# Kernel tuning notes

Hardware: AMD Instinct MI355X
Metric: run time of the kernel (lower is better)

## Reference

```python
import jax, jax.numpy as jnp
import numpy as np

N_IMG, N_CAP, N_REG, N_WORD = 64, 64, 36, 20
EMBED, SIM = 1024, 256
RCAR_STEP = 3          # rar_step=3, rcr_step=2, alv_step=3
T2I_SMOOTH = 9.0
EPS = 1e-8


def l2norm(x):
    return x / (jnp.linalg.norm(x, axis=-1, keepdims=True) + EPS)


def xavier(key, shape):
    fan_in, fan_out = shape[-1], shape[-2]
    r = float(np.sqrt(6.0 / (fan_in + fan_out)))
    return jax.random.uniform(key, shape, jnp.float32, -r, r)


def cross_attention(query, context, matrix, smooth):
    # query: (B, Q, D), context: (B, S, D); matrix broadcasts over query; smooth scalar or (B,Q,1)
    q = query * matrix
    attn = jnp.einsum('bsd,bqd->bsq', context, q)          # (B, S, Q)
    attn = jax.nn.leaky_relu(attn, 0.1)
    attn = l2norm(attn)                                     # normalize over Q
    attn = jnp.swapaxes(attn, 1, 2)                         # (B, Q, S)
    attn = jax.nn.softmax(attn * smooth, axis=2)
    wcontext = jnp.einsum('bqs,bsd->bqd', attn, context)    # (B, Q, D)
    return l2norm(wcontext)


def setup_inputs() -> dict:
    key = jax.random.key(0)
    ks = jax.random.split(key, 12)
    inp = {}
    inp['img_emb'] = jax.random.normal(ks[0], (N_IMG, N_REG, EMBED), jnp.float32)
    inp['cap_emb'] = jax.random.normal(ks[1], (N_CAP, N_WORD, EMBED), jnp.float32)
    inp['cap_lens'] = jnp.full((N_CAP,), N_WORD, dtype=jnp.int32)
    # Alignment_vector: Linear(embed -> sim), 3 steps
    inp['alv_w'] = xavier(ks[2], (RCAR_STEP, SIM, EMBED))
    inp['alv_b'] = jnp.zeros((RCAR_STEP, SIM), jnp.float32)
    # Aggregation_regulator: q/k Linear(sim->sim), v Linear(sim->1), 3 steps
    inp['rar_qw'] = xavier(ks[3], (RCAR_STEP, SIM, SIM))
    inp['rar_qb'] = jnp.zeros((RCAR_STEP, SIM), jnp.float32)
    inp['rar_kw'] = xavier(ks[4], (RCAR_STEP, SIM, SIM))
    inp['rar_kb'] = jnp.zeros((RCAR_STEP, SIM), jnp.float32)
    inp['rar_vw'] = xavier(ks[5], (RCAR_STEP, 1, SIM))
    inp['rar_vb'] = jnp.zeros((RCAR_STEP, 1), jnp.float32)
    # Correpondence_regulator: smooth MLP sim->sim//2->1, matrix MLP sim->2*sim->embed, 2 steps
    inp['rcr_sw1'] = xavier(ks[6], (RCAR_STEP - 1, SIM // 2, SIM))
    inp['rcr_sb1'] = jnp.zeros((RCAR_STEP - 1, SIM // 2), jnp.float32)
    inp['rcr_sw2'] = xavier(ks[7], (RCAR_STEP - 1, 1, SIM // 2))
    inp['rcr_sb2'] = jnp.zeros((RCAR_STEP - 1, 1), jnp.float32)
    inp['rcr_mw1'] = xavier(ks[8], (RCAR_STEP - 1, 2 * SIM, SIM))
    inp['rcr_mb1'] = jnp.zeros((RCAR_STEP - 1, 2 * SIM), jnp.float32)
    inp['rcr_mw2'] = xavier(ks[9], (RCAR_STEP - 1, EMBED, 2 * SIM))
    inp['rcr_mb2'] = jnp.zeros((RCAR_STEP - 1, EMBED), jnp.float32)
    # sim_eval_w: Linear(sim -> 1)
    inp['eval_w'] = xavier(ks[10], (1, SIM))
    inp['eval_b'] = jnp.zeros((1,), jnp.float32)
    return inp


def _forward(img_emb, cap_emb,
             alv_w, alv_b,
             rar_qw, rar_qb, rar_kw, rar_kb, rar_vw, rar_vb,
             rcr_sw1, rcr_sb1, rcr_sw2, rcr_sb2, rcr_mw1, rcr_mb1, rcr_mw2, rcr_mb2,
             eval_w, eval_b):
    n_img = img_emb.shape[0]

    def per_caption(cap_i):                       # cap_i: (L, D)
        query = jnp.broadcast_to(cap_i[None], (n_img,) + cap_i.shape)  # t2i: text is query
        context = img_emb                                               # (n_img, S, D)
        matrix = jnp.ones((EMBED,), cap_i.dtype)
        smooth = jnp.asarray(T2I_SMOOTH, cap_i.dtype)
        sim_hig = None
        for m in range(RCAR_STEP):
            # Alignment_vector (dropout is inference-mode identity)
            wctx = cross_attention(query, context, matrix, smooth)
            sim_rep = (query - wctx) ** 2
            sim_mid = l2norm(jnp.einsum('bqd,sd->bqs', sim_rep, alv_w[m]) + alv_b[m])  # (B,Q,SIM)
            if m == 0:
                sim_hig = sim_mid.mean(axis=1)                                          # (B,SIM)
            if m < RCAR_STEP - 1:
                # Correpondence_regulator
                hm = jnp.tanh(jnp.einsum('bqs,ts->bqt', sim_mid, rcr_mw1[m]) + rcr_mb1[m])
                mm = jnp.einsum('bqt,dt->bqd', hm, rcr_mw2[m]) + rcr_mb2[m]
                matrix = jnp.clip(jnp.tanh(mm) + matrix, -1.0, 1.0)                     # (B,Q,D)
                hs = jnp.tanh(jnp.einsum('bqs,ts->bqt', sim_mid, rcr_sw1[m]) + rcr_sb1[m])
                ss = jnp.einsum('bqt,ot->bqo', hs, rcr_sw2[m]) + rcr_sb2[m]
                smooth = jax.nn.relu(ss + smooth)                                       # (B,Q,1)
            # Aggregation_regulator
            mid_k = jnp.tanh(jnp.einsum('bqs,ts->bqt', sim_mid, rar_kw[m]) + rar_kb[m])
            hig_q = jnp.tanh(sim_hig @ rar_qw[m].T + rar_qb[m])[:, None, :]             # (B,1,SIM)
            w = jnp.einsum('bqs,os->bqo', mid_k * hig_q, rar_vw[m]) + rar_vb[m]         # (B,Q,1)
            w = jax.nn.softmax(w[..., 0], axis=1)
            sim_hig = l2norm(jnp.einsum('bq,bqs->bs', w, sim_mid))
        sim_i = jax.nn.sigmoid(sim_hig @ eval_w.T + eval_b)                             # (B,1)
        return sim_i[:, 0]

    sims = jax.vmap(per_caption)(cap_emb)        # (n_cap, n_img)
    return sims.T                                 # (n_img, n_cap) == torch.cat(sim_all, 1)


def reference(img_emb, cap_emb, cap_lens,
              alv_w, alv_b,
              rar_qw, rar_qb, rar_kw, rar_kb, rar_vw, rar_vb,
              rcr_sw1, rcr_sb1, rcr_sw2, rcr_sb2, rcr_mw1, rcr_mb1, rcr_mw2, rcr_mb2,
              eval_w, eval_b):
    # cap_lens are all equal to N_WORD (constant-length captions), so the per-caption
    # slice cap_emb[i, :n_word] is the full row and the loop vectorizes exactly.
    del cap_lens
    return _forward(img_emb, cap_emb, alv_w, alv_b,
                    rar_qw, rar_qb, rar_kw, rar_kb, rar_vw, rar_vb,
                    rcr_sw1, rcr_sb1, rcr_sw2, rcr_sb2, rcr_mw1, rcr_mb1, rcr_mw2, rcr_mb2,
                    eval_w, eval_b)
```

## Files before the change

### kernel.cpp

```cpp
#include <hip/hip_runtime.h>
#include <math.h>

#define NIMG 64
#define NCAP 64
#define NREG 36
#define NWORD 20
#define EMBED 1024
#define SIMDIM 256
#define H1 512
#define HSD 128
#define EPS 1e-8f

#define QSTR 1032
#define SMSTR 264
#define PSTR 72
#define ATSTR 37

typedef unsigned short u16t;
typedef __bf16 bf8 __attribute__((ext_vector_type(8)));
typedef short  s8i __attribute__((ext_vector_type(8)));
typedef float  f4  __attribute__((ext_vector_type(4)));

__device__ __forceinline__ float wsum(float v) {
#pragma unroll
  for (int o = 32; o > 0; o >>= 1) v += __shfl_xor(v, o);
  return v;
}
__device__ __forceinline__ float wmax(float v) {
#pragma unroll
  for (int o = 32; o > 0; o >>= 1) v = fmaxf(v, __shfl_xor(v, o));
  return v;
}
__device__ __forceinline__ float ftanh(float x) {
  x = fminf(fmaxf(x, -15.f), 15.f);
  float e = __expf(2.f * x);
  return (e - 1.f) / (e + 1.f);
}
__device__ __forceinline__ float d4(float4 a, float4 b) {
  return a.x*b.x + a.y*b.y + a.z*b.z + a.w*b.w;
}
__device__ __forceinline__ u16t f2bf(float f) {
  unsigned u = __float_as_uint(f);
  u += 0x7FFFu + ((u >> 16) & 1u);
  return (u16t)(u >> 16);
}
__device__ __forceinline__ float bf2f(u16t h) { return __uint_as_float(((unsigned)h) << 16); }
__device__ __forceinline__ bf8 zero8() {
  s8i z = {0,0,0,0,0,0,0,0};
  return __builtin_bit_cast(bf8, z);
}
#define MFMA16(a, b, c) __builtin_amdgcn_mfma_f32_16x16x32_bf16((a), (b), (c), 0, 0, 0)

#define WS_ALV   0u
#define WS_KW    786432u
#define WS_MW1   983040u
#define WS_MW2   1245184u
#define WS_SW1   2293760u
#define WS_IMG   2359296u
#define WS_CTXT  4718592u
#define WS_END   8912896u
#define N_CVT    4718592u

#define OFFB_MAT    17825792ull
#define OFFB_SMID   (OFFB_MAT + 83886080ull)
#define OFFB_SHIG   (OFFB_SMID + 41943040ull)
#define OFFB_SMOOTH (OFFB_SHIG + 4194304ull)
#define WS_FULL_BYTES (OFFB_SMOOTH + 327680ull)
#define OFFB_SREP   (OFFB_SMOOTH + 327680ull)
#define OFFB_HQU    (OFFB_SREP + 167772160ull)
#define OFFB_LOG    (OFFB_HQU + 4194304ull)
#define WS_FULL2_BYTES (OFFB_LOG + 327680ull)

__global__ void cvt_kernel(const float* __restrict__ alv, const float* __restrict__ kw,
                           const float* __restrict__ mw1, const float* __restrict__ mw2,
                           const float* __restrict__ sw1, const float* __restrict__ img,
                           u16t* __restrict__ ws) {
  for (unsigned i = blockIdx.x * blockDim.x + threadIdx.x; i < N_CVT; i += gridDim.x * blockDim.x) {
    unsigned o = i; float v;
    if (o < 786432u) v = alv[o];
    else if ((o -= 786432u) < 196608u) v = kw[o];
    else if ((o -= 196608u) < 262144u) v = mw1[o];
    else if ((o -= 262144u) < 1048576u) v = mw2[o];
    else if ((o -= 1048576u) < 65536u) v = sw1[o];
    else { o -= 65536u; v = img[o]; }
    ws[i] = f2bf(v);
  }
}

__global__ void ctxt_kernel(const float* __restrict__ img, u16t* __restrict__ ctxT) {
  __shared__ float tile[36 * 65];
  int b = blockIdx.x;
  int im = b >> 4, dt = (b & 15) * 64;
  const float* src = img + (size_t)im * 36 * 1024 + dt;
  for (int e = threadIdx.x; e < 36 * 64; e += 256) {
    int s = e >> 6, dd = e & 63;
    tile[s * 65 + dd] = src[s * 1024 + dd];
  }
  __syncthreads();
  u16t* dst = ctxT + (size_t)im * 65536 + dt * 64;
  for (int o = threadIdx.x; o < 4096; o += 256) {
    int dd = o >> 6, sp = o & 63;
    dst[dd * 64 + sp] = (sp < 36) ? f2bf(tile[sp * 65 + dd]) : (u16t)0;
  }
}

__global__ __launch_bounds__(512, 4) void simenc_ka(
    const float* __restrict__ cap_emb,
    const u16t* __restrict__ ws,
    const signed char* __restrict__ mat_g,
    const float* __restrict__ smooth_g,
    u16t* __restrict__ srep_g,
    int m)
{
  __shared__ __attribute__((aligned(16))) u16t qsrep[NWORD * QSTR];
  __shared__ __attribute__((aligned(16))) u16t p_bf[NWORD * PSTR];
  __shared__ float attnT[NWORD * ATSTR];
  __shared__ float colscale[36];
  __shared__ float smoothq[NWORD];
  __shared__ float red[8 * NWORD];
  __shared__ float rq[NWORD];

  const int tid = threadIdx.x;
  const int lane = tid & 63;
  const int wv = tid >> 6;
  const int lr = lane & 15;
  const int lg = lane >> 4;
  const int koff = lg * 8;

  const int xcd = blockIdx.x & 7;
  const int j_  = blockIdx.x >> 3;
  const int img = xcd * 8 + (j_ & 7);
  const int cap = j_ >> 3;
  const int pid = img * NCAP + cap;

  const float* qry  = cap_emb + (size_t)cap * (NWORD * EMBED);
  const u16t* imgW  = ws + WS_IMG + (size_t)img * (NREG * EMBED);
  const u16t* ctxTW = ws + WS_CTXT + (size_t)img * (EMBED * 64);

  if (tid < NWORD)
    smoothq[tid] = (m == 0) ? 9.0f : smooth_g[(size_t)pid * 20 + tid];
  __syncthreads();

  if (m == 0) {
#pragma unroll 4
    for (int q = 0; q < NWORD; ++q) {
      qsrep[q * QSTR + tid] = f2bf(qry[q * 1024 + tid]);
      qsrep[q * QSTR + 512 + tid] = f2bf(qry[q * 1024 + 512 + tid]);
    }
  } else {
    const signed char* mg = mat_g + (size_t)pid * 20480;
#pragma unroll 4
    for (int q = 0; q < NWORD; ++q) {
      float mv0 = (float)mg[q * 1024 + tid] * (1.f / 127.f);
      float mv1 = (float)mg[q * 1024 + 512 + tid] * (1.f / 127.f);
      qsrep[q * QSTR + tid] = f2bf(qry[q * 1024 + tid] * mv0);
      qsrep[q * QSTR + 512 + tid] = f2bf(qry[q * 1024 + 512 + tid] * mv1);
    }
  }
  __syncthreads();

  if (wv < 6) {
    int q0 = (wv & 1) * 16, s0 = (wv >> 1) * 16;
    int ari = q0 + lr; bool am = ari >= NWORD; int ar = am ? 0 : ari;
    int bri = s0 + lr; bool bm = bri >= NREG;  int br = bm ? 0 : bri;
    const u16t* ap = qsrep + ar * QSTR + koff;
    const u16t* bp = imgW + (size_t)br * 1024 + koff;
    f4 acc0 = {0.f,0.f,0.f,0.f}, acc1 = {0.f,0.f,0.f,0.f};
#pragma unroll 2
    for (int kk = 0; kk < 32; kk += 2) {
      bf8 a0 = *(const bf8*)(ap + kk * 32);       if (am) a0 = zero8();
      bf8 b0 = *(const bf8*)(bp + kk * 32);       if (bm) b0 = zero8();
      bf8 a1 = *(const bf8*)(ap + (kk + 1) * 32); if (am) a1 = zero8();
      bf8 b1 = *(const bf8*)(bp + (kk + 1) * 32); if (bm) b1 = zero8();
      acc0 = MFMA16(a0, b0, acc0);
      acc1 = MFMA16(a1, b1, acc1);
    }
    f4 acc = acc0 + acc1;
#pragma unroll
    for (int r = 0; r < 4; ++r) {
      int q = q0 + lg * 4 + r, s = s0 + lr;
      if (q < NWORD && s < NREG) {
        float x = acc[r];
        attnT[q * ATSTR + s] = (x > 0.f) ? x : 0.1f * x;
      }
    }
  }
  __syncthreads();

  if (tid < NREG) {
    float ss = 0.f;
#pragma unroll
    for (int q = 0; q < NWORD; ++q) { float v = attnT[q * ATSTR + tid]; ss += v * v; }
    colscale[tid] = 1.f / (sqrtf(ss) + EPS);
  }
  __syncthreads();

#pragma unroll
  for (int pass = 0; pass < 3; ++pass) {
    int q = wv + pass * 8;
    if (q < NWORD) {
      float x = (lane < NREG)
              ? attnT[q * ATSTR + lane] * colscale[lane] * smoothq[q] : -1e30f;
      float mx = wmax(x);
      float e = (lane < NREG) ? __expf(x - mx) : 0.f;
      float s = wsum(e);
      p_bf[q * PSTR + lane] = f2bf(e / s);
    }
  }
  __syncthreads();

  {
    bf8 pa[2][2];
#pragma unroll
    for (int kk = 0; kk < 2; ++kk) {
      pa[0][kk] = *(const bf8*)(p_bf + lr * PSTR + kk * 32 + koff);
      pa[1][kk] = (16 + lr < NWORD)
                ? *(const bf8*)(p_bf + (16 + lr) * PSTR + kk * 32 + koff) : zero8();
    }
    float s2[8];
#pragma unroll
    for (int i = 0; i < 8; ++i) s2[i] = 0.f;
#pragma unroll
    for (int nt = 0; nt < 8; ++nt) {
      int d0 = wv * 128 + nt * 16;
      const u16t* bp = ctxTW + (size_t)(d0 + lr) * 64 + koff;
      bf8 b0 = *(const bf8*)(bp);
      bf8 b1 = *(const bf8*)(bp + 32);
      int d = d0 + lr;
#pragma unroll
      for (int m2 = 0; m2 < 2; ++m2) {
        f4 acc = {0.f,0.f,0.f,0.f};
        acc = MFMA16(pa[m2][0], b0, acc);
        acc = MFMA16(pa[m2][1], b1, acc);
#pragma unroll
        for (int r = 0; r < 4; ++r) {
          int q = m2 * 16 + lg * 4 + r;
          s2[m2 * 4 + r] += acc[r] * acc[r];
          if (q < NWORD) qsrep[q * QSTR + d] = f2bf(acc[r]);
        }
      }
    }
#pragma unroll
    for (int o = 1; o < 16; o <<= 1)
#pragma unroll
      for (int i = 0; i < 8; ++i) s2[i] += __shfl_xor(s2[i], o);
    if (lr == 0) {
#pragma unroll
      for (int r = 0; r < 4; ++r) red[wv * 20 + lg * 4 + r] = s2[r];
      if (lg == 0)
#pragma unroll
        for (int r = 0; r < 4; ++r) red[wv * 20 + 16 + r] = s2[4 + r];
    }
    __syncthreads();
    if (tid < NWORD) {
      float s = 0.f;
#pragma unroll
      for (int w = 0; w < 8; ++w) s += red[w * 20 + tid];
      rq[tid] = 1.f / (sqrtf(s) + EPS);
    }
    __syncthreads();
#pragma unroll
    for (int nt = 0; nt < 8; ++nt) {
      int d = wv * 128 + nt * 16 + lr;
#pragma unroll
      for (int m2 = 0; m2 < 2; ++m2)
#pragma unroll
        for (int r = 0; r < 4; ++r) {
          int q = m2 * 16 + lg * 4 + r;
          if (q < NWORD) {
            float wn = bf2f(qsrep[q * QSTR + d]) * rq[q];
            float t = qry[q * 1024 + d] - wn;
            qsrep[q * QSTR + d] = f2bf(t * t);
          }
        }
    }
  }
  __syncthreads();

  {
    u16t* sp = srep_g + (size_t)pid * 20480;
#pragma unroll 4
    for (int i = tid; i < 20480; i += 512) {
      int row = i >> 10, col = i & 1023;
      sp[i] = qsrep[row * QSTR + col];
    }
  }
}

__global__ __launch_bounds__(1024, 4) void simenc_kf(
    const float* __restrict__ alv_b,
    const u16t* __restrict__ ws,
    const u16t* __restrict__ srep_g,
    u16t* __restrict__ smid_g,
    float* __restrict__ shig_g,
    int m)
{
  __shared__ __attribute__((aligned(16))) u16t smid_l[80 * SMSTR];
  __shared__ float red[16 * 80];
  __shared__ float rq80[80];

  const int tid = threadIdx.x;
  const int lane = tid & 63;
  const int wv = tid >> 6;
  const int lr = lane & 15;
  const int lg = lane >> 4;
  const int koff = lg * 8;

  const int pid0 = blockIdx.x * 4;
  const u16t* alvW = ws + WS_ALV + (size_t)m * (SIMDIM * EMBED);
  const u16t* srepB = srep_g + (size_t)pid0 * 20480;

  int t_ = wv * 16 + lr;
  f4 acc[5];
#pragma unroll
  for (int mt = 0; mt < 5; ++mt) acc[mt] = (f4){0,0,0,0};
#pragma unroll 2
  for (int kk = 0; kk < 32; ++kk) {
    bf8 b = *(const bf8*)(alvW + (size_t)t_ * 1024 + kk * 32 + koff);
#pragma unroll
    for (int mt = 0; mt < 5; ++mt) {
      bf8 a = *(const bf8*)(srepB + (size_t)(mt * 16 + lr) * 1024 + kk * 32 + koff);
      acc[mt] = MFMA16(a, b, acc[mt]);
    }
  }
  float bias = alv_b[m * SIMDIM + t_];
  float p[20];
#pragma unroll
  for (int mt = 0; mt < 5; ++mt)
#pragma unroll
    for (int r = 0; r < 4; ++r) {
      acc[mt][r] += bias;
      p[mt * 4 + r] = acc[mt][r] * acc[mt][r];
    }
#pragma unroll
  for (int o = 1; o < 16; o <<= 1)
#pragma unroll
    for (int i = 0; i < 20; ++i) p[i] += __shfl_xor(p[i], o);
  if (lr == 0)
#pragma unroll
    for (int mt = 0; mt < 5; ++mt)
#pragma unroll
      for (int r = 0; r < 4; ++r)
        red[wv * 80 + mt * 16 + lg * 4 + r] = p[mt * 4 + r];
  __syncthreads();
  if (tid < 80) {
    float s = 0.f;
#pragma unroll
    for (int w = 0; w < 16; ++w) s += red[w * 80 + tid];
    rq80[tid] = 1.f / (sqrtf(s) + EPS);
  }
  __syncthreads();
#pragma unroll
  for (int mt = 0; mt < 5; ++mt)
#pragma unroll
    for (int r = 0; r < 4; ++r) {
      int rb = mt * 16 + lg * 4 + r;
      float v = acc[mt][r] * rq80[rb];
      u16t hv = f2bf(v);
      smid_g[(size_t)(pid0 * 20 + rb) * 256 + t_] = hv;
      smid_l[rb * SMSTR + t_] = hv;
    }
  if (m == 0) {
    __syncthreads();
    int col = tid & 255, pp = tid >> 8;
    float s = 0.f;
#pragma unroll
    for (int q = 0; q < NWORD; ++q) s += bf2f(smid_l[(pp * 20 + q) * SMSTR + col]);
    shig_g[(size_t)(pid0 + pp) * 256 + col] = s * (1.f / NWORD);
  }
}

__global__ __launch_bounds__(1024) void simenc_kh(
    const float* __restrict__ rar_qw, const float* __restrict__ rar_qb,
    const float* __restrict__ rar_vw,
    const float* __restrict__ shig_g, float* __restrict__ hqu_g, int m)
{
  int idx = blockIdx.x * 1024 + threadIdx.x;
  int pid = idx >> 8, t = idx & 255;
  const float4* sh = (const float4*)(shig_g + (size_t)pid * 256);
  const float4* wq = (const float4*)(rar_qw + ((size_t)m * SIMDIM + t) * SIMDIM);
  float acc = 0.f;
#pragma unroll 8
  for (int i = 0; i < SIMDIM / 4; ++i) acc += d4(wq[i], sh[i]);
  hqu_g[idx] = ftanh(acc + rar_qb[m * SIMDIM + t]) * rar_vw[m * SIMDIM + t];
}

__global__ __launch_bounds__(1024, 4) void simenc_kr(
    const float* __restrict__ rar_kb, const float* __restrict__ rar_vb,
    const float* __restrict__ sb1, const float* __restrict__ sw2, const float* __restrict__ sb2,
    const u16t* __restrict__ ws,
    const u16t* __restrict__ smid_g, const float* __restrict__ hqu_g,
    float* __restrict__ logits_g, float* __restrict__ smooth_g,
    int m)
{
  __shared__ float red[16 * 80];

  const int tid = threadIdx.x;
  const int lane = tid & 63;
  const int wv = tid >> 6;
  const int lr = lane & 15;
  const int lg = lane >> 4;
  const int koff = lg * 8;

  const int pid0 = blockIdx.x * 4;
  const u16t* kwW  = ws + WS_KW  + (size_t)m * (SIMDIM * SIMDIM);
  const u16t* sw1W = ws + WS_SW1 + (size_t)m * (HSD * SIMDIM);
  const u16t* smidB = smid_g + (size_t)pid0 * 5120;

  {
    int t_ = wv * 16 + lr;
    f4 acc[5];
#pragma unroll
    for (int mt = 0; mt < 5; ++mt) acc[mt] = (f4){0,0,0,0};
#pragma unroll 2
    for (int kk = 0; kk < 8; ++kk) {
      bf8 b = *(const bf8*)(kwW + (size_t)t_ * 256 + kk * 32 + koff);
#pragma unroll
      for (int mt = 0; mt < 5; ++mt) {
        bf8 a = *(const bf8*)(smidB + (size_t)(mt * 16 + lr) * 256 + kk * 32 + koff);
        acc[mt] = MFMA16(a, b, acc[mt]);
      }
    }
    float kb = rar_kb[m * SIMDIM + t_];
    float p[20];
#pragma unroll
    for (int mt = 0; mt < 5; ++mt)
#pragma unroll
      for (int r = 0; r < 4; ++r) {
        int rb = mt * 16 + lg * 4 + r;
        float hq = hqu_g[(size_t)(pid0 + rb / 20) * 256 + t_];
        p[mt * 4 + r] = ftanh(acc[mt][r] + kb) * hq;
      }
#pragma unroll
    for (int o = 1; o < 16; o <<= 1)
#pragma unroll
      for (int i = 0; i < 20; ++i) p[i] += __shfl_xor(p[i], o);
    if (lr == 0)
#pragma unroll
      for (int mt = 0; mt < 5; ++mt)
#pragma unroll
        for (int r = 0; r < 4; ++r)
          red[wv * 80 + mt * 16 + lg * 4 + r] = p[mt * 4 + r];
  }
  __syncthreads();
  if (tid < 80) {
    float s = 0.f;
#pragma unroll
    for (int w = 0; w < 16; ++w) s += red[w * 80 + tid];
    logits_g[(size_t)pid0 * 20 + tid] = s + rar_vb[m];
  }

  if (m < 2) {
    __syncthreads();
    if (wv < 8) {
      int j_ = wv * 16 + lr;
      f4 acc[5];
#pragma unroll
      for (int mt = 0; mt < 5; ++mt) acc[mt] = (f4){0,0,0,0};
#pragma unroll 2
      for (int kk = 0; kk < 8; ++kk) {
        bf8 b = *(const bf8*)(sw1W + (size_t)j_ * 256 + kk * 32 + koff);
#pragma unroll
        for (int mt = 0; mt < 5; ++mt) {
          bf8 a = *(const bf8*)(smidB + (size_t)(mt * 16 + lr) * 256 + kk * 32 + koff);
          acc[mt] = MFMA16(a, b, acc[mt]);
        }
      }
      float b1 = sb1[m * HSD + j_];
      float s2v = sw2[m * HSD + j_];
      float p[20];
#pragma unroll
      for (int mt = 0; mt < 5; ++mt)
#pragma unroll
        for (int r = 0; r < 4; ++r)
          p[mt * 4 + r] = ftanh(acc[mt][r] + b1) * s2v;
#pragma unroll
      for (int o = 1; o < 16; o <<= 1)
#pragma unroll
        for (int i = 0; i < 20; ++i) p[i] += __shfl_xor(p[i], o);
      if (lr == 0)
#pragma unroll
        for (int mt = 0; mt < 5; ++mt)
#pragma unroll
          for (int r = 0; r < 4; ++r)
            red[wv * 80 + mt * 16 + lg * 4 + r] = p[mt * 4 + r];
    }
    __syncthreads();
    if (tid < 80) {
      float s = 0.f;
#pragma unroll
      for (int w = 0; w < 8; ++w) s += red[w * 80 + tid];
      float old = (m == 0) ? 9.0f : smooth_g[(size_t)pid0 * 20 + tid];
      smooth_g[(size_t)pid0 * 20 + tid] = fmaxf(0.f, s + sb2[m] + old);
    }
  }
}

__global__ __launch_bounds__(256) void simenc_ki(
    const float* __restrict__ eval_w, const float* __restrict__ eval_b,
    const u16t* __restrict__ smid_g, const float* __restrict__ logits_g,
    float* __restrict__ shig_g, float* __restrict__ out, int m)
{
  __shared__ float wsm[NWORD];
  __shared__ float sh[SIMDIM];
  __shared__ float red4[4];
  __shared__ float rsig;

  const int pid = blockIdx.x;
  const int tid = threadIdx.x;

  if (tid < 64) {
    float v = (tid < NWORD) ? logits_g[(size_t)pid * 20 + tid] : -1e30f;
    float mx = wmax(v);
    float e = (tid < NWORD) ? __expf(v - mx) : 0.f;
    float s = wsum(e);
    if (tid < NWORD) wsm[tid] = e / s;
  }
  __syncthreads();
  {
    const u16t* sm = smid_g + (size_t)pid * 5120 + tid;
    float a = 0.f;
#pragma unroll
    for (int q = 0; q < NWORD; ++q) a += wsm[q] * bf2f(sm[q * 256]);
    sh[tid] = a;
  }
  __syncthreads();
  {
    float v = sh[tid];
    float ss = wsum(v * v);
    if ((tid & 63) == 0) red4[tid >> 6] = ss;
  }
  __syncthreads();
  if (tid == 0) rsig = 1.f / (sqrtf(red4[0] + red4[1] + red4[2] + red4[3]) + EPS);
  __syncthreads();
  if (m < 2) {
    shig_g[(size_t)pid * 256 + tid] = sh[tid] * rsig;
  } else if (tid < 64) {
    float4 s4 = ((const float4*)sh)[tid];
    float4 w4 = ((const float4*)eval_w)[tid];
    float v = wsum(d4(s4, w4)) * rsig;
    if (tid == 0) out[pid] = 1.f / (1.f + __expf(-(v + eval_b[0])));
  }
}

__global__ __launch_bounds__(1024, 4) void simenc_k2(
    const float* __restrict__ mb1, const float* __restrict__ mb2,
    const u16t* __restrict__ ws,
    const u16t* __restrict__ smid_g, signed char* __restrict__ mat_g,
    int m)
{
  __shared__ __attribute__((aligned(16))) u16t hm_l[80 * 512];
  __shared__ __attribute__((aligned(16))) signed char mat_l[80 * 1024];

  const int tid = threadIdx.x;
  const int lane = tid & 63;
  const int wv = tid >> 6;
  const int lr = lane & 15;
  const int lg = lane >> 4;
  const int koff = lg * 8;

  const int pid0 = blockIdx.x * 4;
  const u16t* mw1W = ws + WS_MW1 + (size_t)m * (H1 * SIMDIM);
  const u16t* mw2W = ws + WS_MW2 + (size_t)m * (EMBED * H1);
  const u16t* smidB = smid_g + (size_t)pid0 * 5120;

#pragma unroll
  for (int nt = 0; nt < 2; ++nt) {
    int j0 = (wv * 2 + nt) * 16;
    f4 acc[5];
#pragma unroll
    for (int mt = 0; mt < 5; ++mt) acc[mt] = (f4){0,0,0,0};
#pragma unroll 2
    for (int kk = 0; kk < 8; ++kk) {
      bf8 b = *(const bf8*)(mw1W + (size_t)(j0 + lr) * 256 + kk * 32 + koff);
#pragma unroll
      for (int mt = 0; mt < 5; ++mt) {
        bf8 a = *(const bf8*)(smidB + (size_t)(mt * 16 + lr) * 256 + kk * 32 + koff);
        acc[mt] = MFMA16(a, b, acc[mt]);
      }
    }
    int j = j0 + lr;
    float bias = mb1[m * H1 + j];
#pragma unroll
    for (int mt = 0; mt < 5; ++mt)
#pragma unroll
      for (int r = 0; r < 4; ++r) {
        int rb = mt * 16 + lg * 4 + r;
        unsigned byteoff = (unsigned)rb * 1024u
                         + (((unsigned)j * 2u) ^ (((unsigned)rb & 7u) << 4));
        *(u16t*)((char*)hm_l + byteoff) = f2bf(ftanh(acc[mt][r] + bias));
      }
  }
  __syncthreads();

#pragma unroll
  for (int nt = 0; nt < 4; ++nt) {
    int d0 = (wv * 4 + nt) * 16;
    f4 acc[5];
#pragma unroll
    for (int mt = 0; mt < 5; ++mt) acc[mt] = (f4){0,0,0,0};
#pragma unroll 2
    for (int kk = 0; kk < 16; ++kk) {
      bf8 b = *(const bf8*)(mw2W + (size_t)(d0 + lr) * 512 + kk * 32 + koff);
#pragma unroll
      for (int mt = 0; mt < 5; ++mt) {
        int rb = mt * 16 + lr;
        unsigned byteoff = (unsigned)rb * 1024u
                         + (((unsigned)(kk * 64 + lg * 16)) ^ (((unsigned)rb & 7u) << 4));
        bf8 a = *(const bf8*)((const char*)hm_l + byteoff);
        acc[mt] = MFMA16(a, b, acc[mt]);
      }
    }
    int d = d0 + lr;
    float bias = mb2[m * EMBED + d];
#pragma unroll
    for (int mt = 0; mt < 5; ++mt)
#pragma unroll
      for (int r = 0; r < 4; ++r) {
        int rb = mt * 16 + lg * 4 + r;
        float v = ftanh(acc[mt][r] + bias);
        mat_l[rb * 1024 + d] = (signed char)__float2int_rn(v * 127.f);
      }
  }
  __syncthreads();

  {
    signed char* matB = mat_g + (size_t)pid0 * 20480;
#pragma unroll
    for (int i = 0; i < 5; ++i) {
      int off = i * 16384 + tid * 16;
      int4 sv = *(const int4*)(mat_l + off);
      int4 ov;
      if (m > 0) ov = *(const int4*)(matB + off);
      const signed char* svb = (const signed char*)&sv;
      const signed char* ovb = (const signed char*)&ov;
      int4 res;
      signed char* rsb = (signed char*)&res;
#pragma unroll
      for (int b = 0; b < 16; ++b) {
        float v = (float)svb[b] * (1.f / 127.f);
        float mo = (m == 0) ? 1.f : (float)ovb[b] * (1.f / 127.f);
        float mn = fminf(fmaxf(v + mo, -1.f), 1.f);
        rsb[b] = (signed char)__float2int_rn(mn * 127.f);
      }
      *(int4*)(matB + off) = res;
    }
  }
}

__global__ __launch_bounds__(512, 4) void simenc_k1f(
    const float* __restrict__ cap_emb,
    const float* __restrict__ alv_b,
    const float* __restrict__ rar_qw, const float* __restrict__ rar_qb,
    const float* __restrict__ rar_kb,
    const float* __restrict__ rar_vw, const float* __restrict__ rar_vb,
    const float* __restrict__ sb1, const float* __restrict__ sw2, const float* __restrict__ sb2,
    const float* __restrict__ eval_w, const float* __restrict__ eval_b,
    const u16t* __restrict__ ws,
    signed char* __restrict__ mat_g, u16t* __restrict__ smid_g,
    float* __restrict__ shig_g, float* __restrict__ smooth_g,
    int m, float* __restrict__ out)
{
  __shared__ __attribute__((aligned(16))) u16t qsrep[NWORD * QSTR];
  __shared__ __attribute__((aligned(16))) u16t smidb[NWORD * SMSTR];
  __shared__ __attribute__((aligned(16))) u16t p_bf[NWORD * PSTR];
  __shared__ float attnT[NWORD * ATSTR];
  __shared__ float colscale[36];
  __shared__ float smoothq[NWORD];
  __shared__ float sim_hig[SIMDIM];
  __shared__ float red[8 * NWORD];
  __shared__ float rq[NWORD];
  __shared__ float logits_s[NWORD];
  __shared__ float wsm[NWORD];
  __shared__ float ssig_s;

  const int tid = threadIdx.x;
  const int lane = tid & 63;
  const int wv = tid >> 6;
  const int lr = lane & 15;
  const int lg = lane >> 4;
  const int koff = lg * 8;

  const int xcd = blockIdx.x & 7;
  const int j_  = blockIdx.x >> 3;
  const int img = xcd * 8 + (j_ & 7);
  const int cap = j_ >> 3;
  const int pid = img * NCAP + cap;

  const float* qry  = cap_emb + (size_t)cap * (NWORD * EMBED);
  const u16t* imgW  = ws + WS_IMG + (size_t)img * (NREG * EMBED);
  const u16t* ctxTW = ws + WS_CTXT + (size_t)img * (EMBED * 64);
  const u16t* alvW  = ws + WS_ALV + (size_t)m * (SIMDIM * EMBED);
  const u16t* kwW   = ws + WS_KW  + (size_t)m * (SIMDIM * SIMDIM);
  const u16t* sw1W  = ws + WS_SW1 + (size_t)m * (HSD * SIMDIM);

  if (tid < NWORD)
    smoothq[tid] = (m == 0) ? 9.0f : smooth_g[(size_t)pid * 20 + tid];
  if (m > 0 && tid < 256)
    sim_hig[tid] = shig_g[(size_t)pid * 256 + tid];
  __syncthreads();

  if (m == 0) {
#pragma unroll 4
    for (int q = 0; q < NWORD; ++q) {
      qsrep[q * QSTR + tid] = f2bf(qry[q * 1024 + tid]);
      qsrep[q * QSTR + 512 + tid] = f2bf(qry[q * 1024 + 512 + tid]);
    }
  } else {
    const signed char* mg = mat_g + (size_t)pid * 20480;
#pragma unroll 4
    for (int q = 0; q < NWORD; ++q) {
      float mv0 = (float)mg[q * 1024 + tid] * (1.f / 127.f);
      float mv1 = (float)mg[q * 1024 + 512 + tid] * (1.f / 127.f);
      qsrep[q * QSTR + tid] = f2bf(qry[q * 1024 + tid] * mv0);
      qsrep[q * QSTR + 512 + tid] = f2bf(qry[q * 1024 + 512 + tid] * mv1);
    }
  }
  __syncthreads();

  if (wv < 6) {
    int q0 = (wv & 1) * 16, s0 = (wv >> 1) * 16;
    int ari = q0 + lr; bool am = ari >= NWORD; int ar = am ? 0 : ari;
    int bri = s0 + lr; bool bm = bri >= NREG;  int br = bm ? 0 : bri;
    const u16t* ap = qsrep + ar * QSTR + koff;
    const u16t* bp = imgW + (size_t)br * 1024 + koff;
    f4 acc0 = {0.f,0.f,0.f,0.f}, acc1 = {0.f,0.f,0.f,0.f};
#pragma unroll 2
    for (int kk = 0; kk < 32; kk += 2) {
      bf8 a0 = *(const bf8*)(ap + kk * 32);       if (am) a0 = zero8();
      bf8 b0 = *(const bf8*)(bp + kk * 32);       if (bm) b0 = zero8();
      bf8 a1 = *(const bf8*)(ap + (kk + 1) * 32); if (am) a1 = zero8();
      bf8 b1 = *(const bf8*)(bp + (kk + 1) * 32); if (bm) b1 = zero8();
      acc0 = MFMA16(a0, b0, acc0);
      acc1 = MFMA16(a1, b1, acc1);
    }
    f4 acc = acc0 + acc1;
#pragma unroll
    for (int r = 0; r < 4; ++r) {
      int q = q0 + lg * 4 + r, s = s0 + lr;
      if (q < NWORD && s < NREG) {
        float x = acc[r];
        attnT[q * ATSTR + s] = (x > 0.f) ? x : 0.1f * x;
      }
    }
  }
  __syncthreads();

  if (tid < NREG) {
    float ss = 0.f;
#pragma unroll
    for (int q = 0; q < NWORD; ++q) { float v = attnT[q * ATSTR + tid]; ss += v * v; }
    colscale[tid] = 1.f / (sqrtf(ss) + EPS);
  }
  __syncthreads();

#pragma unroll
  for (int pass = 0; pass < 3; ++pass) {
    int q = wv + pass * 8;
    if (q < NWORD) {
      float x = (lane < NREG)
              ? attnT[q * ATSTR + lane] * colscale[lane] * smoothq[q] : -1e30f;
      float mx = wmax(x);
      float e = (lane < NREG) ? __expf(x - mx) : 0.f;
      float s = wsum(e);
      p_bf[q * PSTR + lane] = f2bf(e / s);
    }
  }
  __syncthreads();

  {
    bf8 pa[2][2];
#pragma unroll
    for (int kk = 0; kk < 2; ++kk) {
      pa[0][kk] = *(const bf8*)(p_bf + lr * PSTR + kk * 32 + koff);
      pa[1][kk] = (16 + lr < NWORD)
                ? *(const bf8*)(p_bf + (16 + lr) * PSTR + kk * 32 + koff) : zero8();
    }
    float s2[8];
#pragma unroll
    for (int i = 0; i < 8; ++i) s2[i] = 0.f;
#pragma unroll
    for (int nt = 0; nt < 8; ++nt) {
      int d0 = wv * 128 + nt * 16;
      const u16t* bp = ctxTW + (size_t)(d0 + lr) * 64 + koff;
      bf8 b0 = *(const bf8*)(bp);
      bf8 b1 = *(const bf8*)(bp + 32);
      int d = d0 + lr;
#pragma unroll
      for (int m2 = 0; m2 < 2; ++m2) {
        f4 acc = {0.f,0.f,0.f,0.f};
        acc = MFMA16(pa[m2][0], b0, acc);
        acc = MFMA16(pa[m2][1], b1, acc);
#pragma unroll
        for (int r = 0; r < 4; ++r) {
          int q = m2 * 16 + lg * 4 + r;
          s2[m2 * 4 + r] += acc[r] * acc[r];
          if (q < NWORD) qsrep[q * QSTR + d] = f2bf(acc[r]);
        }
      }
    }
#pragma unroll
    for (int o = 1; o < 16; o <<= 1)
#pragma unroll
      for (int i = 0; i < 8; ++i) s2[i] += __shfl_xor(s2[i], o);
    if (lr == 0) {
#pragma unroll
      for (int r = 0; r < 4; ++r) red[wv * 20 + lg * 4 + r] = s2[r];
      if (lg == 0)
#pragma unroll
        for (int r = 0; r < 4; ++r) red[wv * 20 + 16 + r] = s2[4 + r];
    }
    __syncthreads();
    if (tid < NWORD) {
      float s = 0.f;
#pragma unroll
      for (int w = 0; w < 8; ++w) s += red[w * 20 + tid];
      rq[tid] = 1.f / (sqrtf(s) + EPS);
    }
    __syncthreads();
#pragma unroll
    for (int nt = 0; nt < 8; ++nt) {
      int d = wv * 128 + nt * 16 + lr;
#pragma unroll
      for (int m2 = 0; m2 < 2; ++m2)
#pragma unroll
        for (int r = 0; r < 4; ++r) {
          int q = m2 * 16 + lg * 4 + r;
          if (q < NWORD) {
            float wn = bf2f(qsrep[q * QSTR + d]) * rq[q];
            float t = qry[q * 1024 + d] - wn;
            qsrep[q * QSTR + d] = f2bf(t * t);
          }
        }
    }
  }
  __syncthreads();

  {
    int t0 = wv * 32 + lr;
    const u16t* bp0 = alvW + (size_t)t0 * 1024 + koff;
    const u16t* bp1 = bp0 + 16 * 1024;
    int ari = 16 + lr; bool am = ari >= NWORD; int ar = am ? 0 : ari;
    f4 a00 = {0,0,0,0}, a01 = {0,0,0,0}, a10 = {0,0,0,0}, a11 = {0,0,0,0};
#pragma unroll 2
    for (int kk = 0; kk < 32; ++kk) {
      bf8 b0 = *(const bf8*)(bp0 + kk * 32);
      bf8 b1 = *(const bf8*)(bp1 + kk * 32);
      bf8 x0 = *(const bf8*)(qsrep + lr * QSTR + kk * 32 + koff);
      bf8 x1 = *(const bf8*)(qsrep + ar * QSTR + kk * 32 + koff); if (am) x1 = zero8();
      a00 = MFMA16(x0, b0, a00);
      a01 = MFMA16(x1, b0, a01);
      a10 = MFMA16(x0, b1, a10);
      a11 = MFMA16(x1, b1, a11);
    }
    float bias0 = alv_b[m * SIMDIM + t0];
    float bias1 = alv_b[m * SIMDIM + t0 + 16];
    float s2[8];
#pragma unroll
    for (int r = 0; r < 4; ++r) {
      a00[r] += bias0; a10[r] += bias1;
      s2[r] = a00[r] * a00[r] + a10[r] * a10[r];
    }
#pragma unroll
    for (int r = 0; r < 4; ++r) {
      a01[r] += bias0; a11[r] += bias1;
      s2[4 + r] = (lg == 0) ? a01[r] * a01[r] + a11[r] * a11[r] : 0.f;
    }
#pragma unroll
    for (int o = 1; o < 16; o <<= 1)
#pragma unroll
      for (int i = 0; i < 8; ++i) s2[i] += __shfl_xor(s2[i], o);
    if (lr == 0) {
#pragma unroll
      for (int r = 0; r < 4; ++r) red[wv * 20 + lg * 4 + r] = s2[r];
      if (lg == 0)
#pragma unroll
        for (int r = 0; r < 4; ++r) red[wv * 20 + 16 + r] = s2[4 + r];
    }
    __syncthreads();
    if (tid < NWORD) {
      float s = 0.f;
#pragma unroll
      for (int w = 0; w < 8; ++w) s += red[w * 20 + tid];
      rq[tid] = 1.f / (sqrtf(s) + EPS);
    }
    __syncthreads();
    u16t* sg = smid_g + (size_t)pid * 5120;
#pragma unroll
    for (int r = 0; r < 4; ++r) {
      int q = lg * 4 + r;
      float v0 = a00[r] * rq[q], v1 = a10[r] * rq[q];
      u16t h0 = f2bf(v0), h1 = f2bf(v1);
      ((float*)(qsrep + q * QSTR + 512))[t0] = v0;
      ((float*)(qsrep + q * QSTR + 512))[t0 + 16] = v1;
      smidb[q * SMSTR + t0] = h0;
      smidb[q * SMSTR + t0 + 16] = h1;
      sg[q * 256 + t0] = h0;
      sg[q * 256 + t0 + 16] = h1;
    }
    if (lg == 0)
#pragma unroll
      for (int r = 0; r < 4; ++r) {
        int q = 16 + r;
        float v0 = a01[r] * rq[q], v1 = a11[r] * rq[q];
        u16t h0 = f2bf(v0), h1 = f2bf(v1);
        ((float*)(qsrep + q * QSTR + 512))[t0] = v0;
        ((float*)(qsrep + q * QSTR + 512))[t0 + 16] = v1;
        smidb[q * SMSTR + t0] = h0;
        smidb[q * SMSTR + t0 + 16] = h1;
        sg[q * 256 + t0] = h0;
        sg[q * 256 + t0 + 16] = h1;
      }
  }
  __syncthreads();

  if (m == 0 && tid < 256) {
    float s = 0.f;
#pragma unroll
    for (int q = 0; q < NWORD; ++q) s += ((const float*)(qsrep + q * QSTR + 512))[tid];
    sim_hig[tid] = s * (1.f / NWORD);
  }
  __syncthreads();

  if (m < 2) {
    {
      int j0 = wv * 16;
      int ari = 16 + lr; bool am = ari >= NWORD; int ar = am ? 0 : ari;
      f4 h0 = {0,0,0,0}, h1 = {0,0,0,0};
#pragma unroll 2
      for (int kk = 0; kk < 8; ++kk) {
        bf8 b = *(const bf8*)(sw1W + (size_t)(j0 + lr) * 256 + kk * 32 + koff);
        bf8 x0 = *(const bf8*)(smidb + lr * SMSTR + kk * 32 + koff);
        bf8 x1 = *(const bf8*)(smidb + ar * SMSTR + kk * 32 + koff); if (am) x1 = zero8();
        h0 = MFMA16(x0, b, h0);
        h1 = MFMA16(x1, b, h1);
      }
      int j = j0 + lr;
      float bias = sb1[m * HSD + j];
      float s2v = sw2[m * HSD + j];
      float part[8];
#pragma unroll
      for (int r = 0; r < 4; ++r) part[r] = ftanh(h0[r] + bias) * s2v;
#pragma unroll
      for (int r = 0; r < 4; ++r) part[4 + r] = (lg == 0) ? ftanh(h1[r] + bias) * s2v : 0.f;
#pragma unroll
      for (int o = 1; o < 16; o <<= 1)
#pragma unroll
        for (int i = 0; i < 8; ++i) part[i] += __shfl_xor(part[i], o);
      if (lr == 0) {
#pragma unroll
        for (int r = 0; r < 4; ++r) red[wv * 20 + lg * 4 + r] = part[r];
        if (lg == 0)
#pragma unroll
          for (int r = 0; r < 4; ++r) red[wv * 20 + 16 + r] = part[4 + r];
      }
    }
    __syncthreads();
    if (tid < NWORD) {
      float s = 0.f;
#pragma unroll
      for (int w = 0; w < 8; ++w) s += red[w * 20 + tid];
      smooth_g[(size_t)pid * 20 + tid] = fmaxf(0.f, s + sb2[m] + smoothq[tid]);
    }
    __syncthreads();
  }

  {
    int ari = 16 + lr; bool am = ari >= NWORD; int ar = am ? 0 : ari;
    float part[8];
#pragma unroll
    for (int i = 0; i < 8; ++i) part[i] = 0.f;
#pragma unroll
    for (int h = 0; h < 2; ++h) {
      int t_ = wv * 32 + h * 16 + lr;
      const float4* wq = (const float4*)(rar_qw + ((size_t)m * SIMDIM + t_) * SIMDIM);
      const float4* sh = (const float4*)sim_hig;
      float hacc = 0.f;
#pragma unroll 2
      for (int i = 0; i < SIMDIM / 4; ++i) hacc += d4(wq[i], sh[i]);
      float hq = ftanh(hacc + rar_qb[m * SIMDIM + t_]) * rar_vw[m * SIMDIM + t_];

      f4 k0 = {0,0,0,0}, k1v = {0,0,0,0};
#pragma unroll 2
      for (int kk = 0; kk < 8; ++kk) {
        bf8 b = *(const bf8*)(kwW + (size_t)t_ * 256 + kk * 32 + koff);
        bf8 x0 = *(const bf8*)(smidb + lr * SMSTR + kk * 32 + koff);
        bf8 x1 = *(const bf8*)(smidb + ar * SMSTR + kk * 32 + koff); if (am) x1 = zero8();
        k0 = MFMA16(x0, b, k0);
        k1v = MFMA16(x1, b, k1v);
      }
      float kb = rar_kb[m * SIMDIM + t_];
#pragma unroll
      for (int r = 0; r < 4; ++r) part[r] += ftanh(k0[r] + kb) * hq;
      if (lg == 0)
#pragma unroll
        for (int r = 0; r < 4; ++r) part[4 + r] += ftanh(k1v[r] + kb) * hq;
    }
#pragma unroll
    for (int o = 1; o < 16; o <<= 1)
#pragma unroll
      for (int i = 0; i < 8; ++i) part[i] += __shfl_xor(part[i], o);
    if (lr == 0) {
#pragma unroll
      for (int r = 0; r < 4; ++r) red[wv * 20 + lg * 4 + r] = part[r];
      if (lg == 0)
#pragma unroll
        for (int r = 0; r < 4; ++r) red[wv * 20 + 16 + r] = part[4 + r];
    }
  }
  __syncthreads();
  if (tid < NWORD) {
    float s = 0.f;
#pragma unroll
    for (int w = 0; w < 8; ++w) s += red[w * 20 + tid];
    logits_s[tid] = s + rar_vb[m];
  }
  __syncthreads();
  if (tid < 64) {
    float v = (tid < NWORD) ? logits_s[tid] : -1e30f;
    float mx = wmax(v);
    float e = (tid < NWORD) ? __expf(v - mx) : 0.f;
    float s = wsum(e);
    if (tid < NWORD) wsm[tid] = e / s;
  }
  __syncthreads();
  if (tid < 256) {
    float a = 0.f;
#pragma unroll
    for (int q = 0; q < NWORD; ++q) a += wsm[q] * ((const float*)(qsrep + q * QSTR + 512))[tid];
    sim_hig[tid] = a;
  }
  __syncthreads();
  if (tid < 64) {
    float4 v = ((const float4*)sim_hig)[tid];
    float s = wsum(d4(v, v));
    if (tid == 0) ssig_s = 1.f / (sqrtf(s) + EPS);
  }
  __syncthreads();

  if (m < 2) {
    if (tid < 256)
      shig_g[(size_t)pid * 256 + tid] = sim_hig[tid] * ssig_s;
  } else {
    if (tid < 64) {
      float4 s4v = ((const float4*)sim_hig)[tid];
      float4 w4v = ((const float4*)eval_w)[tid];
      float v = wsum(d4(s4v, w4v)) * ssig_s;
      if (tid == 0)
        out[pid] = 1.f / (1.f + __expf(-(v + eval_b[0])));
    }
  }
}

extern "C" void kernel_launch(void* const* d_in, const int* in_sizes, int n_in,
                              void* d_out, int out_size, void* d_ws, size_t ws_size,
                              hipStream_t stream) {
  (void)in_sizes; (void)n_in; (void)out_size;
  u16t* ws = (u16t*)d_ws;

  signed char* mat_g = (signed char*)d_ws + OFFB_MAT;
  u16t*  smid_g   = (u16t*)((char*)d_ws + OFFB_SMID);
  float* shig_g   = (float*)((char*)d_ws + OFFB_SHIG);
  float* smooth_g = (float*)((char*)d_ws + OFFB_SMOOTH);

  cvt_kernel<<<2048, 1024, 0, stream>>>(
      (const float*)d_in[3],  (const float*)d_in[7],  (const float*)d_in[15],
      (const float*)d_in[17], (const float*)d_in[11], (const float*)d_in[0], ws);
  ctxt_kernel<<<1024, 256, 0, stream>>>((const float*)d_in[0], ws + WS_CTXT);

  if (ws_size >= (size_t)WS_FULL2_BYTES) {
    u16t*  srep_g   = (u16t*)((char*)d_ws + OFFB_SREP);
    float* hqu_g    = (float*)((char*)d_ws + OFFB_HQU);
    float* logits_g = (float*)((char*)d_ws + OFFB_LOG);

    for (int m = 0; m < 3; ++m) {
      simenc_ka<<<NIMG * NCAP, 512, 0, stream>>>(
          (const float*)d_in[1], ws, mat_g, smooth_g, srep_g, m);
      simenc_kf<<<NIMG * NCAP / 4, 1024, 0, stream>>>(
          (const float*)d_in[4], ws, srep_g, smid_g, shig_g, m);
      simenc_kh<<<1024, 1024, 0, stream>>>(
          (const float*)d_in[5], (const float*)d_in[6], (const float*)d_in[9],
          shig_g, hqu_g, m);
      simenc_kr<<<NIMG * NCAP / 4, 1024, 0, stream>>>(
          (const float*)d_in[8], (const float*)d_in[10],
          (const float*)d_in[12], (const float*)d_in[13], (const float*)d_in[14],
          ws, smid_g, hqu_g, logits_g, smooth_g, m);
      simenc_ki<<<NIMG * NCAP, 256, 0, stream>>>(
          (const float*)d_in[19], (const float*)d_in[20],
          smid_g, logits_g, shig_g, (float*)d_out, m);
      if (m < 2)
        simenc_k2<<<NIMG * NCAP / 4, 1024, 0, stream>>>(
            (const float*)d_in[16], (const float*)d_in[18],
            ws, smid_g, mat_g, m);
    }
  } else {
    for (int m = 0; m < 3; ++m) {
      simenc_k1f<<<NIMG * NCAP, 512, 0, stream>>>(
          (const float*)d_in[1],  (const float*)d_in[4],
          (const float*)d_in[5],  (const float*)d_in[6],  (const float*)d_in[8],
          (const float*)d_in[9],  (const float*)d_in[10],
          (const float*)d_in[12], (const float*)d_in[13], (const float*)d_in[14],
          (const float*)d_in[19], (const float*)d_in[20],
          ws, mat_g, smid_g, shig_g, smooth_g, m, (float*)d_out);
      if (m < 2)
        simenc_k2<<<NIMG * NCAP / 4, 1024, 0, stream>>>(
            (const float*)d_in[16], (const float*)d_in[18],
            ws, smid_g, mat_g, m);
    }
  }
}
```

Measured before the change: 3.513 ms.

## Fuse per-step pipeline into one persistent kernel with global scratch for query rep

Replaces the five-kernel per-step chain (ka, kf, kh, kr, ki) with one fused kernel, simenc_k1g. It launches 1024 blocks, and each block loops over 4 image-caption pairs, computing attention, the alignment vector, the smooth MLP, the regulator and the final sigmoid in one pass. The large shared query buffer is moved to a per-block global scratch area (srep_g). This frees shared memory for fp32 and bf16 sim_mid tiles and lets launch bounds rise to 8 blocks per CU. It removes kernel launches and global round trips for intermediates, at the cost of global-memory traffic for the query/residual buffer and heavier per-block serial work.

```diff
diff --git a/kernel.cpp b/kernel.cpp
--- a/kernel.cpp
+++ b/kernel.cpp
@@ -66,10 +66,8 @@
 #define OFFB_SHIG   (OFFB_SMID + 41943040ull)
 #define OFFB_SMOOTH (OFFB_SHIG + 4194304ull)
 #define WS_FULL_BYTES (OFFB_SMOOTH + 327680ull)
-#define OFFB_SREP   (OFFB_SMOOTH + 327680ull)
-#define OFFB_HQU    (OFFB_SREP + 167772160ull)
-#define OFFB_LOG    (OFFB_HQU + 4194304ull)
-#define WS_FULL2_BYTES (OFFB_LOG + 327680ull)
+#define OFFB_SREP   WS_FULL_BYTES
+#define WS_TIER_A   (OFFB_SREP + 41943040ull)
 
 __global__ void cvt_kernel(const float* __restrict__ alv, const float* __restrict__ kw,
                            const float* __restrict__ mw1, const float* __restrict__ mw2,
@@ -104,21 +102,32 @@
   }
 }
 
-__global__ __launch_bounds__(512, 4) void simenc_ka(
+__global__ __launch_bounds__(512, 8) void simenc_k1g(
     const float* __restrict__ cap_emb,
+    const float* __restrict__ alv_b,
+    const float* __restrict__ rar_qw, const float* __restrict__ rar_qb,
+    const float* __restrict__ rar_kb,
+    const float* __restrict__ rar_vw, const float* __restrict__ rar_vb,
+    const float* __restrict__ sb1, const float* __restrict__ sw2, const float* __restrict__ sb2,
+    const float* __restrict__ eval_w, const float* __restrict__ eval_b,
     const u16t* __restrict__ ws,
-    const signed char* __restrict__ mat_g,
-    const float* __restrict__ smooth_g,
+    signed char* __restrict__ mat_g, u16t* __restrict__ smid_g,
+    float* __restrict__ shig_g, float* __restrict__ smooth_g,
     u16t* __restrict__ srep_g,
-    int m)
+    int m, float* __restrict__ out)
 {
-  __shared__ __attribute__((aligned(16))) u16t qsrep[NWORD * QSTR];
+  __shared__ float smidf[NWORD * 256];
+  __shared__ __attribute__((aligned(16))) u16t smidb[NWORD * SMSTR];
   __shared__ __attribute__((aligned(16))) u16t p_bf[NWORD * PSTR];
   __shared__ float attnT[NWORD * ATSTR];
   __shared__ float colscale[36];
   __shared__ float smoothq[NWORD];
+  __shared__ float sim_hig[SIMDIM];
   __shared__ float red[8 * NWORD];
   __shared__ float rq[NWORD];
+  __shared__ float logits_s[NWORD];
+  __shared__ float wsm[NWORD];
+  __shared__ float ssig_s;
 
   const int tid = threadIdx.x;
   const int lane = tid & 63;
@@ -127,523 +136,374 @@
   const int lg = lane >> 4;
   const int koff = lg * 8;
 
-  const int xcd = blockIdx.x & 7;
-  const int j_  = blockIdx.x >> 3;
-  const int img = xcd * 8 + (j_ & 7);
-  const int cap = j_ >> 3;
-  const int pid = img * NCAP + cap;
-
-  const float* qry  = cap_emb + (size_t)cap * (NWORD * EMBED);
-  const u16t* imgW  = ws + WS_IMG + (size_t)img * (NREG * EMBED);
-  const u16t* ctxTW = ws + WS_CTXT + (size_t)img * (EMBED * 64);
-
-  if (tid < NWORD)
-    smoothq[tid] = (m == 0) ? 9.0f : smooth_g[(size_t)pid * 20 + tid];
-  __syncthreads();
-
-  if (m == 0) {
+  u16t* srp = srep_g + (size_t)blockIdx.x * 20480;
+
+  for (int c = 0; c < 4; ++c) {
+    int v = blockIdx.x + (c << 10);
+    int xcd = v & 7, j_ = v >> 3;
+    int img = xcd * 8 + (j_ & 7);
+    int cap = j_ >> 3;
+    int pid = img * NCAP + cap;
+
+    const float* qry  = cap_emb + (size_t)cap * (NWORD * EMBED);
+    const u16t* imgW  = ws + WS_IMG + (size_t)img * (NREG * EMBED);
+    const u16t* ctxTW = ws + WS_CTXT + (size_t)img * (EMBED * 64);
+    const u16t* alvW  = ws + WS_ALV + (size_t)m * (SIMDIM * EMBED);
+    const u16t* kwW   = ws + WS_KW  + (size_t)m * (SIMDIM * SIMDIM);
+    const u16t* sw1W  = ws + WS_SW1 + (size_t)m * (HSD * SIMDIM);
+
+    __syncthreads();
+    if (tid < NWORD)
+      smoothq[tid] = (m == 0) ? 9.0f : smooth_g[(size_t)pid * 20 + tid];
+    if (m > 0 && tid < 256)
+      sim_hig[tid] = shig_g[(size_t)pid * 256 + tid];
+
+    {
+      int c0 = tid * 2;
+      if (m == 0) {
 #pragma unroll 4
-    for (int q = 0; q < NWORD; ++q) {
-      qsrep[q * QSTR + tid] = f2bf(qry[q * 1024 + tid]);
-      qsrep[q * QSTR + 512 + tid] = f2bf(qry[q * 1024 + 512 + tid]);
-    }
-  } else {
-    const signed char* mg = mat_g + (size_t)pid * 20480;
+        for (int q = 0; q < NWORD; ++q) {
+          float2 qv = *(const float2*)(qry + q * 1024 + c0);
+          unsigned pk = (unsigned)f2bf(qv.x) | ((unsigned)f2bf(qv.y) << 16);
+          *(unsigned*)(srp + q * 1024 + c0) = pk;
+        }
+      } else {
+        const signed char* mg = mat_g + (size_t)pid * 20480;
 #pragma unroll 4
-    for (int q = 0; q < NWORD; ++q) {
-      float mv0 = (float)mg[q * 1024 + tid] * (1.f / 127.f);
-      float mv1 = (float)mg[q * 1024 + 512 + tid] * (1.f / 127.f);
-      qsrep[q * QSTR + tid] = f2bf(qry[q * 1024 + tid] * mv0);
-      qsrep[q * QSTR + 512 + tid] = f2bf(qry[q * 1024 + 512 + tid] * mv1);
-    }
-  }
-  __syncthreads();
-
-  if (wv < 6) {
-    int q0 = (wv & 1) * 16, s0 = (wv >> 1) * 16;
-    int ari = q0 + lr; bool am = ari >= NWORD; int ar = am ? 0 : ari;
-    int bri = s0 + lr; bool bm = bri >= NREG;  int br = bm ? 0 : bri;
-    const u16t* ap = qsrep + ar * QSTR + koff;
-    const u16t* bp = imgW + (size_t)br * 1024 + koff;
-    f4 acc0 = {0.f,0.f,0.f,0.f}, acc1 = {0.f,0.f,0.f,0.f};
-#pragma unroll 2
-    for (int kk = 0; kk < 32; kk += 2) {
-      bf8 a0 = *(const bf8*)(ap + kk * 32);       if (am) a0 = zero8();
-      bf8 b0 = *(const bf8*)(bp + kk * 32);       if (bm) b0 = zero8();
-      bf8 a1 = *(const bf8*)(ap + (kk + 1) * 32); if (am) a1 = zero8();
-      bf8 b1 = *(const bf8*)(bp + (kk + 1) * 32); if (bm) b1 = zero8();
-      acc0 = MFMA16(a0, b0, acc0);
-      acc1 = MFMA16(a1, b1, acc1);
-    }
-    f4 acc = acc0 + acc1;
-#pragma unroll
-    for (int r = 0; r < 4; ++r) {
-      int q = q0 + lg * 4 + r, s = s0 + lr;
-      if (q < NWORD && s < NREG) {
-        float x = acc[r];
-        attnT[q * ATSTR + s] = (x > 0.f) ? x : 0.1f * x;
-      }
-    }
-  }
-  __syncthreads();
-
-  if (tid < NREG) {
-    float ss = 0.f;
-#pragma unroll
-    for (int q = 0; q < NWORD; ++q) { float v = attnT[q * ATSTR + tid]; ss += v * v; }
-    colscale[tid] = 1.f / (sqrtf(ss) + EPS);
-  }
-  __syncthreads();
-
-#pragma unroll
-  for (int pass = 0; pass < 3; ++pass) {
-    int q = wv + pass * 8;
-    if (q < NWORD) {
-      float x = (lane < NREG)
-              ? attnT[q * ATSTR + lane] * colscale[lane] * smoothq[q] : -1e30f;
-      float mx = wmax(x);
-      float e = (lane < NREG) ? __expf(x - mx) : 0.f;
-      float s = wsum(e);
-      p_bf[q * PSTR + lane] = f2bf(e / s);
-    }
-  }
-  __syncthreads();
-
-  {
-    bf8 pa[2][2];
-#pragma unroll
-    for (int kk = 0; kk < 2; ++kk) {
-      pa[0][kk] = *(const bf8*)(p_bf + lr * PSTR + kk * 32 + koff);
-      pa[1][kk] = (16 + lr < NWORD)
-                ? *(const bf8*)(p_bf + (16 + lr) * PSTR + kk * 32 + koff) : zero8();
-    }
-    float s2[8];
-#pragma unroll
-    for (int i = 0; i < 8; ++i) s2[i] = 0.f;
-#pragma unroll
-    for (int nt = 0; nt < 8; ++nt) {
-      int d0 = wv * 128 + nt * 16;
-      const u16t* bp = ctxTW + (size_t)(d0 + lr) * 64 + koff;
-      bf8 b0 = *(const bf8*)(bp);
-      bf8 b1 = *(const bf8*)(bp + 32);
-      int d = d0 + lr;
-#pragma unroll
-      for (int m2 = 0; m2 < 2; ++m2) {
-        f4 acc = {0.f,0.f,0.f,0.f};
-        acc = MFMA16(pa[m2][0], b0, acc);
-        acc = MFMA16(pa[m2][1], b1, acc);
+        for (int q = 0; q < NWORD; ++q) {
+          float2 qv = *(const float2*)(qry + q * 1024 + c0);
+          float m0 = (float)mg[q * 1024 + c0] * (1.f / 127.f);
+          float m1 = (float)mg[q * 1024 + c0 + 1] * (1.f / 127.f);
+          unsigned pk = (unsigned)f2bf(qv.x * m0) | ((unsigned)f2bf(qv.y * m1) << 16);
+          *(unsigned*)(srp + q * 1024 + c0) = pk;
+        }
+      }
+    }
+    __syncthreads();
+
+    if (wv < 6) {
+      int q0 = (wv & 1) * 16, s0 = (wv >> 1) * 16;
+      int ari = q0 + lr; bool am = ari >= NWORD; int ar = am ? 0 : ari;
+      int bri = s0 + lr; bool bm = bri >= NREG;  int br = bm ? 0 : bri;
+      const u16t* ap = srp + ar * 1024 + koff;
+      const u16t* bp = imgW + (size_t)br * 1024 + koff;
+      f4 acc0 = {0.f,0.f,0.f,0.f}, acc1 = {0.f,0.f,0.f,0.f};
+      for (int kk = 0; kk < 32; kk += 2) {
+        bf8 a0 = *(const bf8*)(ap + kk * 32);       if (am) a0 = zero8();
+        bf8 b0 = *(const bf8*)(bp + kk * 32);       if (bm) b0 = zero8();
+        bf8 a1 = *(const bf8*)(ap + (kk + 1) * 32); if (am) a1 = zero8();
+        bf8 b1 = *(const bf8*)(bp + (kk + 1) * 32); if (bm) b1 = zero8();
+        acc0 = MFMA16(a0, b0, acc0);
+        acc1 = MFMA16(a1, b1, acc1);
+      }
+      f4 acc = acc0 + acc1;
+#pragma unroll
+      for (int r = 0; r < 4; ++r) {
+        int q = q0 + lg * 4 + r, s = s0 + lr;
+        if (q < NWORD && s < NREG) {
+          float x = acc[r];
+          attnT[q * ATSTR + s] = (x > 0.f) ? x : 0.1f * x;
+        }
+      }
+    }
+    __syncthreads();
+
+    if (tid < NREG) {
+      float ss = 0.f;
+#pragma unroll
+      for (int q = 0; q < NWORD; ++q) { float vv = attnT[q * ATSTR + tid]; ss += vv * vv; }
+      colscale[tid] = 1.f / (sqrtf(ss) + EPS);
+    }
+    __syncthreads();
+
+#pragma unroll
+    for (int pass = 0; pass < 3; ++pass) {
+      int q = wv + pass * 8;
+      if (q < NWORD) {
+        float x = (lane < NREG)
+                ? attnT[q * ATSTR + lane] * colscale[lane] * smoothq[q] : -1e30f;
+        float mx = wmax(x);
+        float e = (lane < NREG) ? __expf(x - mx) : 0.f;
+        float s = wsum(e);
+        p_bf[q * PSTR + lane] = f2bf(e / s);
+      }
+    }
+    __syncthreads();
+
+    {
+      bf8 pa[2][2];
+#pragma unroll
+      for (int kk = 0; kk < 2; ++kk) {
+        pa[0][kk] = *(const bf8*)(p_bf + lr * PSTR + kk * 32 + koff);
+        pa[1][kk] = (16 + lr < NWORD)
+                  ? *(const bf8*)(p_bf + (16 + lr) * PSTR + kk * 32 + koff) : zero8();
+      }
+      float s2[8];
+#pragma unroll
+      for (int i = 0; i < 8; ++i) s2[i] = 0.f;
+      for (int nt = 0; nt < 8; ++nt) {
+        int d0 = wv * 128 + nt * 16;
+        const u16t* bp = ctxTW + (size_t)(d0 + lr) * 64 + koff;
+        bf8 b0 = *(const bf8*)(bp);
+        bf8 b1 = *(const bf8*)(bp + 32);
+        int d = d0 + lr;
+#pragma unroll
+        for (int m2 = 0; m2 < 2; ++m2) {
+          f4 acc = {0.f,0.f,0.f,0.f};
+          acc = MFMA16(pa[m2][0], b0, acc);
+          acc = MFMA16(pa[m2][1], b1, acc);
+#pragma unroll
+          for (int r = 0; r < 4; ++r) {
+            int q = m2 * 16 + lg * 4 + r;
+            s2[m2 * 4 + r] += acc[r] * acc[r];
+            if (q < NWORD) srp[q * 1024 + d] = f2bf(acc[r]);
+          }
+        }
+      }
+#pragma unroll
+      for (int o = 1; o < 16; o <<= 1)
+#pragma unroll
+        for (int i = 0; i < 8; ++i) s2[i] += __shfl_xor(s2[i], o);
+      if (lr == 0) {
+#pragma unroll
+        for (int r = 0; r < 4; ++r) red[wv * 20 + lg * 4 + r] = s2[r];
+        if (lg == 0)
+#pragma unroll
+          for (int r = 0; r < 4; ++r) red[wv * 20 + 16 + r] = s2[4 + r];
+      }
+      __syncthreads();
+      if (tid < NWORD) {
+        float s = 0.f;
+#pragma unroll
+        for (int w = 0; w < 8; ++w) s += red[w * 20 + tid];
+        rq[tid] = 1.f / (sqrtf(s) + EPS);
+      }
+      __syncthreads();
+      for (int nt = 0; nt < 8; ++nt) {
+        int d = wv * 128 + nt * 16 + lr;
+#pragma unroll
+        for (int m2 = 0; m2 < 2; ++m2)
+#pragma unroll
+          for (int r = 0; r < 4; ++r) {
+            int q = m2 * 16 + lg * 4 + r;
+            if (q < NWORD) {
+              float wn = bf2f(srp[q * 1024 + d]) * rq[q];
+              float t = qry[q * 1024 + d] - wn;
+              srp[q * 1024 + d] = f2bf(t * t);
+            }
+          }
+      }
+    }
+    __syncthreads();
+
+    {
+      int t0 = wv * 32 + lr;
+      const u16t* bp0 = alvW + (size_t)t0 * 1024 + koff;
+      const u16t* bp1 = bp0 + 16 * 1024;
+      int ari = 16 + lr; bool am = ari >= NWORD; int ar = am ? 0 : ari;
+      f4 a00 = {0,0,0,0}, a01 = {0,0,0,0}, a10 = {0,0,0,0}, a11 = {0,0,0,0};
+      for (int kk = 0; kk < 32; ++kk) {
+        bf8 b0 = *(const bf8*)(bp0 + kk * 32);
+        bf8 b1 = *(const bf8*)(bp1 + kk * 32);
+        bf8 x0 = *(const bf8*)(srp + lr * 1024 + kk * 32 + koff);
+        bf8 x1 = *(const bf8*)(srp + ar * 1024 + kk * 32 + koff); if (am) x1 = zero8();
+        a00 = MFMA16(x0, b0, a00);
+        a01 = MFMA16(x1, b0, a01);
+        a10 = MFMA16(x0, b1, a10);
+        a11 = MFMA16(x1, b1, a11);
+      }
+      float bias0 = alv_b[m * SIMDIM + t0];
+      float bias1 = alv_b[m * SIMDIM + t0 + 16];
+      float s2[8];
+#pragma unroll
+      for (int r = 0; r < 4; ++r) {
+        a00[r] += bias0; a10[r] += bias1;
+        s2[r] = a00[r] * a00[r] + a10[r] * a10[r];
+      }
+#pragma unroll
+      for (int r = 0; r < 4; ++r) {
+        a01[r] += bias0; a11[r] += bias1;
+        s2[4 + r] = (lg == 0) ? a01[r] * a01[r] + a11[r] * a11[r] : 0.f;
+      }
+#pragma unroll
+      for (int o = 1; o < 16; o <<= 1)
+#pragma unroll
+        for (int i = 0; i < 8; ++i) s2[i] += __shfl_xor(s2[i], o);
+      if (lr == 0) {
+#pragma unroll
+        for (int r = 0; r < 4; ++r) red[wv * 20 + lg * 4 + r] = s2[r];
+        if (lg == 0)
+#pragma unroll
+          for (int r = 0; r < 4; ++r) red[wv * 20 + 16 + r] = s2[4 + r];
+      }
+      __syncthreads();
+      if (tid < NWORD) {
+        float s = 0.f;
+#pragma unroll
+        for (int w = 0; w < 8; ++w) s += red[w * 20 + tid];
+        rq[tid] = 1.f / (sqrtf(s) + EPS);
+      }
+      __syncthreads();
+      u16t* sg = smid_g + (size_t)pid * 5120;
+#pragma unroll
+      for (int r = 0; r < 4; ++r) {
+        int q = lg * 4 + r;
+        float v0 = a00[r] * rq[q], v1 = a10[r] * rq[q];
+        u16t h0 = f2bf(v0), h1 = f2bf(v1);
+        smidf[q * 256 + t0] = v0;
+        smidf[q * 256 + t0 + 16] = v1;
+        smidb[q * SMSTR + t0] = h0;
+        smidb[q * SMSTR + t0 + 16] = h1;
+        sg[q * 256 + t0] = h0;
+        sg[q * 256 + t0 + 16] = h1;
+      }
+      if (lg == 0)
 #pragma unroll
         for (int r = 0; r < 4; ++r) {
-          int q = m2 * 16 + lg * 4 + r;
-          s2[m2 * 4 + r] += acc[r] * acc[r];
-          if (q < NWORD) qsrep[q * QSTR + d] = f2bf(acc[r]);
+          int q = 16 + r;
+          float v0 = a01[r] * rq[q], v1 = a11[r] * rq[q];
+          u16t h0 = f2bf(v0), h1 = f2bf(v1);
+          smidf[q * 256 + t0] = v0;
+          smidf[q * 256 + t0 + 16] = v1;
+          smidb[q * SMSTR + t0] = h0;
+          smidb[q * SMSTR + t0 + 16] = h1;
+          sg[q * 256 + t0] = h0;
+          sg[q * 256 + t0 + 16] = h1;
         }
-      }
-    }
-#pragma unroll
-    for (int o = 1; o < 16; o <<= 1)
-#pragma unroll
-      for (int i = 0; i < 8; ++i) s2[i] += __shfl_xor(s2[i], o);
-    if (lr == 0) {
-#pragma unroll
-      for (int r = 0; r < 4; ++r) red[wv * 20 + lg * 4 + r] = s2[r];
-      if (lg == 0)
-#pragma unroll
-        for (int r = 0; r < 4; ++r) red[wv * 20 + 16 + r] = s2[4 + r];
+    }
+    __syncthreads();
+
+    if (m == 0 && tid < 256) {
+      float s = 0.f;
+#pragma unroll
+      for (int q = 0; q < NWORD; ++q) s += smidf[q * 256 + tid];
+      sim_hig[tid] = s * (1.f / NWORD);
+    }
+    __syncthreads();
+
+    if (m < 2) {
+      {
+        int j0 = wv * 16;
+        int ari = 16 + lr; bool am = ari >= NWORD; int ar = am ? 0 : ari;
+        f4 h0 = {0,0,0,0}, h1 = {0,0,0,0};
+        for (int kk = 0; kk < 8; ++kk) {
+          bf8 b = *(const bf8*)(sw1W + (size_t)(j0 + lr) * 256 + kk * 32 + koff);
+          bf8 x0 = *(const bf8*)(smidb + lr * SMSTR + kk * 32 + koff);
+          bf8 x1 = *(const bf8*)(smidb + ar * SMSTR + kk * 32 + koff); if (am) x1 = zero8();
+          h0 = MFMA16(x0, b, h0);
+          h1 = MFMA16(x1, b, h1);
+        }
+        int j = j0 + lr;
+        float bias = sb1[m * HSD + j];
+        float s2v = sw2[m * HSD + j];
+        float part[8];
+#pragma unroll
+        for (int r = 0; r < 4; ++r) part[r] = ftanh(h0[r] + bias) * s2v;
+#pragma unroll
+        for (int r = 0; r < 4; ++r) part[4 + r] = (lg == 0) ? ftanh(h1[r] + bias) * s2v : 0.f;
+#pragma unroll
+        for (int o = 1; o < 16; o <<= 1)
+#pragma unroll
+          for (int i = 0; i < 8; ++i) part[i] += __shfl_xor(part[i], o);
+        if (lr == 0) {
+#pragma unroll
+          for (int r = 0; r < 4; ++r) red[wv * 20 + lg * 4 + r] = part[r];
+          if (lg == 0)
+#pragma unroll
+            for (int r = 0; r < 4; ++r) red[wv * 20 + 16 + r] = part[4 + r];
+        }
+      }
+      __syncthreads();
+      if (tid < NWORD) {
+        float s = 0.f;
+#pragma unroll
+        for (int w = 0; w < 8; ++w) s += red[w * 20 + tid];
+        smooth_g[(size_t)pid * 20 + tid] = fmaxf(0.f, s + sb2[m] + smoothq[tid]);
+      }
+      __syncthreads();
+    }
+
+    {
+      int ari = 16 + lr; bool am = ari >= NWORD; int ar = am ? 0 : ari;
+      float part[8];
+#pragma unroll
+      for (int i = 0; i < 8; ++i) part[i] = 0.f;
+      for (int h = 0; h < 2; ++h) {
+        int t_ = wv * 32 + h * 16 + lr;
+        const float4* wq = (const float4*)(rar_qw + ((size_t)m * SIMDIM + t_) * SIMDIM);
+        const float4* sh = (const float4*)sim_hig;
+        float hacc = 0.f;
+        for (int i = 0; i < SIMDIM / 4; ++i) hacc += d4(wq[i], sh[i]);
+        float hq = ftanh(hacc + rar_qb[m * SIMDIM + t_]) * rar_vw[m * SIMDIM + t_];
+
+        f4 k0 = {0,0,0,0}, k1v = {0,0,0,0};
+        for (int kk = 0; kk < 8; ++kk) {
+          bf8 b = *(const bf8*)(kwW + (size_t)t_ * 256 + kk * 32 + koff);
+          bf8 x0 = *(const bf8*)(smidb + lr * SMSTR + kk * 32 + koff);
+          bf8 x1 = *(const bf8*)(smidb + ar * SMSTR + kk * 32 + koff); if (am) x1 = zero8();
+          k0 = MFMA16(x0, b, k0);
+          k1v = MFMA16(x1, b, k1v);
+        }
+        float kb = rar_kb[m * SIMDIM + t_];
+#pragma unroll
+        for (int r = 0; r < 4; ++r) part[r] += ftanh(k0[r] + kb) * hq;
+        if (lg == 0)
+#pragma unroll
+          for (int r = 0; r < 4; ++r) part[4 + r] += ftanh(k1v[r] + kb) * hq;
+      }
+#pragma unroll
+      for (int o = 1; o < 16; o <<= 1)
+#pragma unroll
+        for (int i = 0; i < 8; ++i) part[i] += __shfl_xor(part[i], o);
+      if (lr == 0) {
+#pragma unroll
+        for (int r = 0; r < 4; ++r) red[wv * 20 + lg * 4 + r] = part[r];
+        if (lg == 0)
+#pragma unroll
+          for (int r = 0; r < 4; ++r) red[wv * 20 + 16 + r] = part[4 + r];
+      }
     }
     __syncthreads();
     if (tid < NWORD) {
       float s = 0.f;
 #pragma unroll
       for (int w = 0; w < 8; ++w) s += red[w * 20 + tid];
-      rq[tid] = 1.f / (sqrtf(s) + EPS);
-    }
-    __syncthreads();
-#pragma unroll
-    for (int nt = 0; nt < 8; ++nt) {
-      int d = wv * 128 + nt * 16 + lr;
-#pragma unroll
-      for (int m2 = 0; m2 < 2; ++m2)
-#pragma unroll
-        for (int r = 0; r < 4; ++r) {
-          int q = m2 * 16 + lg * 4 + r;
-          if (q < NWORD) {
-            float wn = bf2f(qsrep[q * QSTR + d]) * rq[q];
-            float t = qry[q * 1024 + d] - wn;
-            qsrep[q * QSTR + d] = f2bf(t * t);
-          }
-        }
-    }
-  }
-  __syncthreads();
-
-  {
-    u16t* sp = srep_g + (size_t)pid * 20480;
-#pragma unroll 4
-    for (int i = tid; i < 20480; i += 512) {
-      int row = i >> 10, col = i & 1023;
-      sp[i] = qsrep[row * QSTR + col];
-    }
-  }
-}
-
-__global__ __launch_bounds__(1024, 4) void simenc_kf(
-    const float* __restrict__ alv_b,
-    const u16t* __restrict__ ws,
-    const u16t* __restrict__ srep_g,
-    u16t* __restrict__ smid_g,
-    float* __restrict__ shig_g,
-    int m)
-{
-  __shared__ __attribute__((aligned(16))) u16t smid_l[80 * SMSTR];
-  __shared__ float red[16 * 80];
-  __shared__ float rq80[80];
-
-  const int tid = threadIdx.x;
-  const int lane = tid & 63;
-  const int wv = tid >> 6;
-  const int lr = lane & 15;
-  const int lg = lane >> 4;
-  const int koff = lg * 8;
-
-  const int pid0 = blockIdx.x * 4;
-  const u16t* alvW = ws + WS_ALV + (size_t)m * (SIMDIM * EMBED);
-  const u16t* srepB = srep_g + (size_t)pid0 * 20480;
-
-  int t_ = wv * 16 + lr;
-  f4 acc[5];
-#pragma unroll
-  for (int mt = 0; mt < 5; ++mt) acc[mt] = (f4){0,0,0,0};
-#pragma unroll 2
-  for (int kk = 0; kk < 32; ++kk) {
-    bf8 b = *(const bf8*)(alvW + (size_t)t_ * 1024 + kk * 32 + koff);
-#pragma unroll
-    for (int mt = 0; mt < 5; ++mt) {
-      bf8 a = *(const bf8*)(srepB + (size_t)(mt * 16 + lr) * 1024 + kk * 32 + koff);
-      acc[mt] = MFMA16(a, b, acc[mt]);
-    }
-  }
-  float bias = alv_b[m * SIMDIM + t_];
-  float p[20];
-#pragma unroll
-  for (int mt = 0; mt < 5; ++mt)
-#pragma unroll
-    for (int r = 0; r < 4; ++r) {
-      acc[mt][r] += bias;
-      p[mt * 4 + r] = acc[mt][r] * acc[mt][r];
-    }
-#pragma unroll
-  for (int o = 1; o < 16; o <<= 1)
-#pragma unroll
-    for (int i = 0; i < 20; ++i) p[i] += __shfl_xor(p[i], o);
-  if (lr == 0)
-#pragma unroll
-    for (int mt = 0; mt < 5; ++mt)
-#pragma unroll
-      for (int r = 0; r < 4; ++r)
-        red[wv * 80 + mt * 16 + lg * 4 + r] = p[mt * 4 + r];
-  __syncthreads();
-  if (tid < 80) {
-    float s = 0.f;
-#pragma unroll
-    for (int w = 0; w < 16; ++w) s += red[w * 80 + tid];
-    rq80[tid] = 1.f / (sqrtf(s) + EPS);
-  }
-  __syncthreads();
-#pragma unroll
-  for (int mt = 0; mt < 5; ++mt)
-#pragma unroll
-    for (int r = 0; r < 4; ++r) {
-      int rb = mt * 16 + lg * 4 + r;
-      float v = acc[mt][r] * rq80[rb];
-      u16t hv = f2bf(v);
-      smid_g[(size_t)(pid0 * 20 + rb) * 256 + t_] = hv;
-      smid_l[rb * SMSTR + t_] = hv;
-    }
-  if (m == 0) {
-    __syncthreads();
-    int col = tid & 255, pp = tid >> 8;
-    float s = 0.f;
-#pragma unroll
-    for (int q = 0; q < NWORD; ++q) s += bf2f(smid_l[(pp * 20 + q) * SMSTR + col]);
-    shig_g[(size_t)(pid0 + pp) * 256 + col] = s * (1.f / NWORD);
-  }
-}
-
-__global__ __launch_bounds__(1024) void simenc_kh(
-    const float* __restrict__ rar_qw, const float* __restrict__ rar_qb,
-    const float* __restrict__ rar_vw,
-    const float* __restrict__ shig_g, float* __restrict__ hqu_g, int m)
-{
-  int idx = blockIdx.x * 1024 + threadIdx.x;
-  int pid = idx >> 8, t = idx & 255;
-  const float4* sh = (const float4*)(shig_g + (size_t)pid * 256);
-  const float4* wq = (const float4*)(rar_qw + ((size_t)m * SIMDIM + t) * SIMDIM);
-  float acc = 0.f;
-#pragma unroll 8
-  for (int i = 0; i < SIMDIM / 4; ++i) acc += d4(wq[i], sh[i]);
-  hqu_g[idx] = ftanh(acc + rar_qb[m * SIMDIM + t]) * rar_vw[m * SIMDIM + t];
-}
-
-__global__ __launch_bounds__(1024, 4) void simenc_kr(
-    const float* __restrict__ rar_kb, const float* __restrict__ rar_vb,
-    const float* __restrict__ sb1, const float* __restrict__ sw2, const float* __restrict__ sb2,
-    const u16t* __restrict__ ws,
-    const u16t* __restrict__ smid_g, const float* __restrict__ hqu_g,
-    float* __restrict__ logits_g, float* __restrict__ smooth_g,
-    int m)
-{
-  __shared__ float red[16 * 80];
-
-  const int tid = threadIdx.x;
-  const int lane = tid & 63;
-  const int wv = tid >> 6;
-  const int lr = lane & 15;
-  const int lg = lane >> 4;
-  const int koff = lg * 8;
-
-  const int pid0 = blockIdx.x * 4;
-  const u16t* kwW  = ws + WS_KW  + (size_t)m * (SIMDIM * SIMDIM);
-  const u16t* sw1W = ws + WS_SW1 + (size_t)m * (HSD * SIMDIM);
-  const u16t* smidB = smid_g + (size_t)pid0 * 5120;
-
-  {
-    int t_ = wv * 16 + lr;
-    f4 acc[5];
-#pragma unroll
-    for (int mt = 0; mt < 5; ++mt) acc[mt] = (f4){0,0,0,0};
-#pragma unroll 2
-    for (int kk = 0; kk < 8; ++kk) {
-      bf8 b = *(const bf8*)(kwW + (size_t)t_ * 256 + kk * 32 + koff);
-#pragma unroll
-      for (int mt = 0; mt < 5; ++mt) {
-        bf8 a = *(const bf8*)(smidB + (size_t)(mt * 16 + lr) * 256 + kk * 32 + koff);
-        acc[mt] = MFMA16(a, b, acc[mt]);
-      }
-    }
-    float kb = rar_kb[m * SIMDIM + t_];
-    float p[20];
-#pragma unroll
-    for (int mt = 0; mt < 5; ++mt)
-#pragma unroll
-      for (int r = 0; r < 4; ++r) {
-        int rb = mt * 16 + lg * 4 + r;
-        float hq = hqu_g[(size_t)(pid0 + rb / 20) * 256 + t_];
-        p[mt * 4 + r] = ftanh(acc[mt][r] + kb) * hq;
-      }
-#pragma unroll
-    for (int o = 1; o < 16; o <<= 1)
-#pragma unroll
-      for (int i = 0; i < 20; ++i) p[i] += __shfl_xor(p[i], o);
-    if (lr == 0)
-#pragma unroll
-      for (int mt = 0; mt < 5; ++mt)
-#pragma unroll
-        for (int r = 0; r < 4; ++r)
-          red[wv * 80 + mt * 16 + lg * 4 + r] = p[mt * 4 + r];
-  }
-  __syncthreads();
-  if (tid < 80) {
-    float s = 0.f;
-#pragma unroll
-    for (int w = 0; w < 16; ++w) s += red[w * 80 + tid];
-    logits_g[(size_t)pid0 * 20 + tid] = s + rar_vb[m];
-  }
-
-  if (m < 2) {
-    __syncthreads();
-    if (wv < 8) {
-      int j_ = wv * 16 + lr;
-      f4 acc[5];
-#pragma unroll
-      for (int mt = 0; mt < 5; ++mt) acc[mt] = (f4){0,0,0,0};
-#pragma unroll 2
-      for (int kk = 0; kk < 8; ++kk) {
-        bf8 b = *(const bf8*)(sw1W + (size_t)j_ * 256 + kk * 32 + koff);
-#pragma unroll
-        for (int mt = 0; mt < 5; ++mt) {
-          bf8 a = *(const bf8*)(smidB + (size_t)(mt * 16 + lr) * 256 + kk * 32 + koff);
-          acc[mt] = MFMA16(a, b, acc[mt]);
-        }
-      }
-      float b1 = sb1[m * HSD + j_];
-      float s2v = sw2[m * HSD + j_];
-      float p[20];
-#pragma unroll
-      for (int mt = 0; mt < 5; ++mt)
-#pragma unroll
-        for (int r = 0; r < 4; ++r)
-          p[mt * 4 + r] = ftanh(acc[mt][r] + b1) * s2v;
-#pragma unroll
-      for (int o = 1; o < 16; o <<= 1)
-#pragma unroll
-        for (int i = 0; i < 20; ++i) p[i] += __shfl_xor(p[i], o);
-      if (lr == 0)
-#pragma unroll
-        for (int mt = 0; mt < 5; ++mt)
-#pragma unroll
-          for (int r = 0; r < 4; ++r)
-            red[wv * 80 + mt * 16 + lg * 4 + r] = p[mt * 4 + r];
-    }
-    __syncthreads();
-    if (tid < 80) {
-      float s = 0.f;
-#pragma unroll
-      for (int w = 0; w < 8; ++w) s += red[w * 80 + tid];
-      float old = (m == 0) ? 9.0f : smooth_g[(size_t)pid0 * 20 + tid];
-      smooth_g[(size_t)pid0 * 20 + tid] = fmaxf(0.f, s + sb2[m] + old);
-    }
-  }
-}
-
-__global__ __launch_bounds__(256) void simenc_ki(
-    const float* __restrict__ eval_w, const float* __restrict__ eval_b,
-    const u16t* __restrict__ smid_g, const float* __restrict__ logits_g,
-    float* __restrict__ shig_g, float* __restrict__ out, int m)
-{
-  __shared__ float wsm[NWORD];
-  __shared__ float sh[SIMDIM];
-  __shared__ float red4[4];
-  __shared__ float rsig;
-
-  const int pid = blockIdx.x;
-  const int tid = threadIdx.x;
-
-  if (tid < 64) {
-    float v = (tid < NWORD) ? logits_g[(size_t)pid * 20 + tid] : -1e30f;
-    float mx = wmax(v);
-    float e = (tid < NWORD) ? __expf(v - mx) : 0.f;
-    float s = wsum(e);
-    if (tid < NWORD) wsm[tid] = e / s;
-  }
-  __syncthreads();
-  {
-    const u16t* sm = smid_g + (size_t)pid * 5120 + tid;
-    float a = 0.f;
-#pragma unroll
-    for (int q = 0; q < NWORD; ++q) a += wsm[q] * bf2f(sm[q * 256]);
-    sh[tid] = a;
-  }
-  __syncthreads();
-  {
-    float v = sh[tid];
-    float ss = wsum(v * v);
-    if ((tid & 63) == 0) red4[tid >> 6] = ss;
-  }
-  __syncthreads();
-  if (tid == 0) rsig = 1.f / (sqrtf(red4[0] + red4[1] + red4[2] + red4[3]) + EPS);
-  __syncthreads();
-  if (m < 2) {
-    shig_g[(size_t)pid * 256 + tid] = sh[tid] * rsig;
-  } else if (tid < 64) {
-    float4 s4 = ((const float4*)sh)[tid];
-    float4 w4 = ((const float4*)eval_w)[tid];
-    float v = wsum(d4(s4, w4)) * rsig;
-    if (tid == 0) out[pid] = 1.f / (1.f + __expf(-(v + eval_b[0])));
-  }
-}
-
-__global__ __launch_bounds__(1024, 4) void simenc_k2(
-    const float* __restrict__ mb1, const float* __restrict__ mb2,
-    const u16t* __restrict__ ws,
-    const u16t* __restrict__ smid_g, signed char* __restrict__ mat_g,
-    int m)
-{
-  __shared__ __attribute__((aligned(16))) u16t hm_l[80 * 512];
-  __shared__ __attribute__((aligned(16))) signed char mat_l[80 * 1024];
-
-  const int tid = threadIdx.x;
-  const int lane = tid & 63;
-  const int wv = tid >> 6;
-  const int lr = lane & 15;
-  const int lg = lane >> 4;
-  const int koff = lg * 8;
-
-  const int pid0 = blockIdx.x * 4;
-  const u16t* mw1W = ws + WS_MW1 + (size_t)m * (H1 * SIMDIM);
-  const u16t* mw2W = ws + WS_MW2 + (size_t)m * (EMBED * H1);
-  const u16t* smidB = smid_g + (size_t)pid0 * 5120;
-
-#pragma unroll
-  for (int nt = 0; nt < 2; ++nt) {
-    int j0 = (wv * 2 + nt) * 16;
-    f4 acc[5];
-#pragma unroll
-    for (int mt = 0; mt < 5; ++mt) acc[mt] = (f4){0,0,0,0};
-#pragma unroll 2
-    for (int kk = 0; kk < 8; ++kk) {
-      bf8 b = *(const bf8*)(mw1W + (size_t)(j0 + lr) * 256 + kk * 32 + koff);
-#pragma unroll
-      for (int mt = 0; mt < 5; ++mt) {
-        bf8 a = *(const bf8*)(smidB + (size_t)(mt * 16 + lr) * 256 + kk * 32 + koff);
-        acc[mt] = MFMA16(a, b, acc[mt]);
-      }
-    }
-    int j = j0 + lr;
-    float bias = mb1[m * H1 + j];
-#pragma unroll
-    for (int mt = 0; mt < 5; ++mt)
-#pragma unroll
-      for (int r = 0; r < 4; ++r) {
-        int rb = mt * 16 + lg * 4 + r;
-        unsigned byteoff = (unsigned)rb * 1024u
-                         + (((unsigned)j * 2u) ^ (((unsigned)rb & 7u) << 4));
-        *(u16t*)((char*)hm_l + byteoff) = f2bf(ftanh(acc[mt][r] + bias));
-      }
-  }
-  __syncthreads();
-
-#pragma unroll
-  for (int nt = 0; nt < 4; ++nt) {
-    int d0 = (wv * 4 + nt) * 16;
-    f4 acc[5];
-#pragma unroll
-    for (int mt = 0; mt < 5; ++mt) acc[mt] = (f4){0,0,0,0};
-#pragma unroll 2
-    for (int kk = 0; kk < 16; ++kk) {
-      bf8 b = *(const bf8*)(mw2W + (size_t)(d0 + lr) * 512 + kk * 32 + koff);
-#pragma unroll
-      for (int mt = 0; mt < 5; ++mt) {
-        int rb = mt * 16 + lr;
-        unsigned byteoff = (unsigned)rb * 1024u
-                         + (((unsigned)(kk * 64 + lg * 16)) ^ (((unsigned)rb & 7u) << 4));
-        bf8 a = *(const bf8*)((const char*)hm_l + byteoff);
-        acc[mt] = MFMA16(a, b, acc[mt]);
-      }
-    }
-    int d = d0 + lr;
-    float bias = mb2[m * EMBED + d];
-#pragma unroll
-    for (int mt = 0; mt < 5; ++mt)
-#pragma unroll
-      for (int r = 0; r < 4; ++r) {
-        int rb = mt * 16 + lg * 4 + r;
-        float v = ftanh(acc[mt][r] + bias);
-        mat_l[rb * 1024 + d] = (signed char)__float2int_rn(v * 127.f);
-      }
-  }
-  __syncthreads();
-
-  {
-    signed char* matB = mat_g + (size_t)pid0 * 20480;
-#pragma unroll
-    for (int i = 0; i < 5; ++i) {
-      int off = i * 16384 + tid * 16;
-      int4 sv = *(const int4*)(mat_l + off);
-      int4 ov;
-      if (m > 0) ov = *(const int4*)(matB + off);
-      const signed char* svb = (const signed char*)&sv;
-      const signed char* ovb = (const signed char*)&ov;
-      int4 res;
-      signed char* rsb = (signed char*)&res;
-#pragma unroll
-      for (int b = 0; b < 16; ++b) {
-        float v = (float)svb[b] * (1.f / 127.f);
-        float mo = (m == 0) ? 1.f : (float)ovb[b] * (1.f / 127.f);
-        float mn = fminf(fmaxf(v + mo, -1.f), 1.f);
-        rsb[b] = (signed char)__float2int_rn(mn * 127.f);
-      }
-      *(int4*)(matB + off) = res;
+      logits_s[tid] = s + rar_vb[m];
+    }
+    __syncthreads();
+    if (tid < 64) {
+      float vv = (tid < NWORD) ? logits_s[tid] : -1e30f;
+      float mx = wmax(vv);
+      float e = (tid < NWORD) ? __expf(vv - mx) : 0.f;
+      float s = wsum(e);
+      if (tid < NWORD) wsm[tid] = e / s;
+    }
+    __syncthreads();
+    if (tid < 256) {
+      float a = 0.f;
+#pragma unroll
+      for (int q = 0; q < NWORD; ++q) a += wsm[q] * smidf[q * 256 + tid];
+      sim_hig[tid] = a;
+    }
+    __syncthreads();
+    if (tid < 64) {
+      float4 vv = ((const float4*)sim_hig)[tid];
+      float s = wsum(d4(vv, vv));
+      if (tid == 0) ssig_s = 1.f / (sqrtf(s) + EPS);
+    }
+    __syncthreads();
+
+    if (m < 2) {
+      if (tid < 256)
+        shig_g[(size_t)pid * 256 + tid] = sim_hig[tid] * ssig_s;
+    } else {
+      if (tid < 64) {
+        float4 s4v = ((const float4*)sim_hig)[tid];
+        float4 w4v = ((const float4*)eval_w)[tid];
+        float vv = wsum(d4(s4v, w4v)) * ssig_s;
+        if (tid == 0)
+          out[pid] = 1.f / (1.f + __expf(-(vv + eval_b[0])));
+      }
     }
   }
 }
@@ -749,7 +609,7 @@
   if (tid < NREG) {
     float ss = 0.f;
 #pragma unroll
-    for (int q = 0; q < NWORD; ++q) { float v = attnT[q * ATSTR + tid]; ss += v * v; }
+    for (int q = 0; q < NWORD; ++q) { float vv = attnT[q * ATSTR + tid]; ss += vv * vv; }
     colscale[tid] = 1.f / (sqrtf(ss) + EPS);
   }
   __syncthreads();
@@ -1017,9 +877,9 @@
   }
   __syncthreads();
   if (tid < 64) {
-    float v = (tid < NWORD) ? logits_s[tid] : -1e30f;
-    float mx = wmax(v);
-    float e = (tid < NWORD) ? __expf(v - mx) : 0.f;
+    float vv = (tid < NWORD) ? logits_s[tid] : -1e30f;
+    float mx = wmax(vv);
+    float e = (tid < NWORD) ? __expf(vv - mx) : 0.f;
     float s = wsum(e);
     if (tid < NWORD) wsm[tid] = e / s;
   }
@@ -1032,8 +892,8 @@
   }
   __syncthreads();
   if (tid < 64) {
-    float4 v = ((const float4*)sim_hig)[tid];
-    float s = wsum(d4(v, v));
+    float4 vv = ((const float4*)sim_hig)[tid];
+    float s = wsum(d4(vv, vv));
     if (tid == 0) ssig_s = 1.f / (sqrtf(s) + EPS);
   }
   __syncthreads();
@@ -1045,9 +905,114 @@
     if (tid < 64) {
       float4 s4v = ((const float4*)sim_hig)[tid];
       float4 w4v = ((const float4*)eval_w)[tid];
-      float v = wsum(d4(s4v, w4v)) * ssig_s;
+      float vv = wsum(d4(s4v, w4v)) * ssig_s;
       if (tid == 0)
-        out[pid] = 1.f / (1.f + __expf(-(v + eval_b[0])));
+        out[pid] = 1.f / (1.f + __expf(-(vv + eval_b[0])));
+    }
+  }
+}
+
+__global__ __launch_bounds__(1024, 4) void simenc_k2(
+    const float* __restrict__ mb1, const float* __restrict__ mb2,
+    const u16t* __restrict__ ws,
+    const u16t* __restrict__ smid_g, signed char* __restrict__ mat_g,
+    int m)
+{
+  __shared__ __attribute__((aligned(16))) u16t hm_l[80 * 512];
+  __shared__ __attribute__((aligned(16))) signed char mat_l[80 * 1024];
+
+  const int tid = threadIdx.x;
+  const int lane = tid & 63;
+  const int wv = tid >> 6;
+  const int lr = lane & 15;
+  const int lg = lane >> 4;
+  const int koff = lg * 8;
+
+  const int pid0 = blockIdx.x * 4;
+  const u16t* mw1W = ws + WS_MW1 + (size_t)m * (H1 * SIMDIM);
+  const u16t* mw2W = ws + WS_MW2 + (size_t)m * (EMBED * H1);
+  const u16t* smidB = smid_g + (size_t)pid0 * 5120;
+
+#pragma unroll
+  for (int nt = 0; nt < 2; ++nt) {
+    int j0 = (wv * 2 + nt) * 16;
+    f4 acc[5];
+#pragma unroll
+    for (int mt = 0; mt < 5; ++mt) acc[mt] = (f4){0,0,0,0};
+#pragma unroll 2
+    for (int kk = 0; kk < 8; ++kk) {
+      bf8 b = *(const bf8*)(mw1W + (size_t)(j0 + lr) * 256 + kk * 32 + koff);
+#pragma unroll
+      for (int mt = 0; mt < 5; ++mt) {
+        bf8 a = *(const bf8*)(smidB + (size_t)(mt * 16 + lr) * 256 + kk * 32 + koff);
+        acc[mt] = MFMA16(a, b, acc[mt]);
+      }
+    }
+    int j = j0 + lr;
+    float bias = mb1[m * H1 + j];
+#pragma unroll
+    for (int mt = 0; mt < 5; ++mt)
+#pragma unroll
+      for (int r = 0; r < 4; ++r) {
+        int rb = mt * 16 + lg * 4 + r;
+        unsigned byteoff = (unsigned)rb * 1024u
+                         + (((unsigned)j * 2u) ^ (((unsigned)rb & 7u) << 4));
+        *(u16t*)((char*)hm_l + byteoff) = f2bf(ftanh(acc[mt][r] + bias));
+      }
+  }
+  __syncthreads();
+
+#pragma unroll
+  for (int nt = 0; nt < 4; ++nt) {
+    int d0 = (wv * 4 + nt) * 16;
+    f4 acc[5];
+#pragma unroll
+    for (int mt = 0; mt < 5; ++mt) acc[mt] = (f4){0,0,0,0};
+#pragma unroll 2
+    for (int kk = 0; kk < 16; ++kk) {
+      bf8 b = *(const bf8*)(mw2W + (size_t)(d0 + lr) * 512 + kk * 32 + koff);
+#pragma unroll
+      for (int mt = 0; mt < 5; ++mt) {
+        int rb = mt * 16 + lr;
+        unsigned byteoff = (unsigned)rb * 1024u
+                         + (((unsigned)(kk * 64 + lg * 16)) ^ (((unsigned)rb & 7u) << 4));
+        bf8 a = *(const bf8*)((const char*)hm_l + byteoff);
+        acc[mt] = MFMA16(a, b, acc[mt]);
+      }
+    }
+    int d = d0 + lr;
+    float bias = mb2[m * EMBED + d];
+#pragma unroll
+    for (int mt = 0; mt < 5; ++mt)
+#pragma unroll
+      for (int r = 0; r < 4; ++r) {
+        int rb = mt * 16 + lg * 4 + r;
+        float v = ftanh(acc[mt][r] + bias);
+        mat_l[rb * 1024 + d] = (signed char)__float2int_rn(v * 127.f);
+      }
+  }
+  __syncthreads();
+
+  {
+    signed char* matB = mat_g + (size_t)pid0 * 20480;
+#pragma unroll
+    for (int i = 0; i < 5; ++i) {
+      int off = i * 16384 + tid * 16;
+      int4 sv = *(const int4*)(mat_l + off);
+      int4 ov;
+      if (m > 0) ov = *(const int4*)(matB + off);
+      const signed char* svb = (const signed char*)&sv;
+      const signed char* ovb = (const signed char*)&ov;
+      int4 res;
+      signed char* rsb = (signed char*)&res;
+#pragma unroll
+      for (int b = 0; b < 16; ++b) {
+        float v = (float)svb[b] * (1.f / 127.f);
+        float mo = (m == 0) ? 1.f : (float)ovb[b] * (1.f / 127.f);
+        float mn = fminf(fmaxf(v + mo, -1.f), 1.f);
+        rsb[b] = (signed char)__float2int_rn(mn * 127.f);
+      }
+      *(int4*)(matB + off) = res;
     }
   }
 }
@@ -1068,26 +1033,16 @@
       (const float*)d_in[17], (const float*)d_in[11], (const float*)d_in[0], ws);
   ctxt_kernel<<<1024, 256, 0, stream>>>((const float*)d_in[0], ws + WS_CTXT);
 
-  if (ws_size >= (size_t)WS_FULL2_BYTES) {
-    u16t*  srep_g   = (u16t*)((char*)d_ws + OFFB_SREP);
-    float* hqu_g    = (float*)((char*)d_ws + OFFB_HQU);
-    float* logits_g = (float*)((char*)d_ws + OFFB_LOG);
-
+  if (ws_size >= (size_t)WS_TIER_A) {
+    u16t* srep_g = (u16t*)((char*)d_ws + OFFB_SREP);
     for (int m = 0; m < 3; ++m) {
-      simenc_ka<<<NIMG * NCAP, 512, 0, stream>>>(
-          (const float*)d_in[1], ws, mat_g, smooth_g, srep_g, m);
-      simenc_kf<<<NIMG * NCAP / 4, 1024, 0, stream>>>(
-          (const float*)d_in[4], ws, srep_g, smid_g, shig_g, m);
-      simenc_kh<<<1024, 1024, 0, stream>>>(
-          (const float*)d_in[5], (const float*)d_in[6], (const float*)d_in[9],
-          shig_g, hqu_g, m);
-      simenc_kr<<<NIMG * NCAP / 4, 1024, 0, stream>>>(
-          (const float*)d_in[8], (const float*)d_in[10],
+      simenc_k1g<<<1024, 512, 0, stream>>>(
+          (const float*)d_in[1],  (const float*)d_in[4],
+          (const float*)d_in[5],  (const float*)d_in[6],  (const float*)d_in[8],
+          (const float*)d_in[9],  (const float*)d_in[10],
           (const float*)d_in[12], (const float*)d_in[13], (const float*)d_in[14],
-          ws, smid_g, hqu_g, logits_g, smooth_g, m);
-      simenc_ki<<<NIMG * NCAP, 256, 0, stream>>>(
           (const float*)d_in[19], (const float*)d_in[20],
-          smid_g, logits_g, shig_g, (float*)d_out, m);
+          ws, mat_g, smid_g, shig_g, smooth_g, srep_g, m, (float*)d_out);
       if (m < 2)
         simenc_k2<<<NIMG * NCAP / 4, 1024, 0, stream>>>(
             (const float*)d_in[16], (const float*)d_in[18],
```

New measurement: 9.062 ms. 158% more time.
